# Kernel tuning notes

Hardware: AMD Instinct MI355X
Metric: run time of the kernel (lower is better)

Reference implementation:

```python
import jax, jax.numpy as jnp
import numpy as np

N, E, G = 2048, 65536, 32
F_ATOM, LAT, IN, ED, NB, L = 16, 64, 128, 32, 5, 5


def setup_inputs() -> dict:
    key = jax.random.key(0)
    ks = iter(jax.random.split(key, 64))
    nxt = lambda: next(ks)
    def w(shape):
        fan_in = shape[-2] if len(shape) >= 2 else 1
        return jax.random.normal(nxt(), shape, jnp.float32) / np.sqrt(fan_in)
    inp = {}
    inp['x'] = jax.random.normal(nxt(), (N, F_ATOM), jnp.float32)
    inp['t'] = jax.random.uniform(nxt(), (G, 1), jnp.float32)
    inp['z'] = jax.random.normal(nxt(), (N, LAT), jnp.float32)
    inp['edge_index'] = jax.random.randint(nxt(), (2, E), 0, N, jnp.int32)
    inp['edge_attr'] = jax.random.normal(nxt(), (E, NB), jnp.float32)
    inp['batch'] = jnp.sort(jax.random.randint(nxt(), (N,), 0, G, jnp.int32))
    inp['batch_edge_global'] = jax.random.randint(nxt(), (E,), 0, G, jnp.int32)
    # top-level dense layers
    inp['Wt_a'] = w((1, IN)); inp['bt_a'] = jnp.zeros((IN,))
    inp['Wt_b'] = w((1, ED)); inp['bt_b'] = jnp.zeros((ED,))
    inp['W_atom'] = w((F_ATOM, IN)); inp['b_atom'] = jnp.zeros((IN,))
    inp['W_bond'] = w((NB, ED)); inp['b_bond'] = jnp.zeros((ED,))
    inp['W_lat'] = w((LAT, IN)); inp['b_lat'] = jnp.zeros((IN,))
    inp['W_at'] = w((IN, IN)); inp['b_at'] = jnp.zeros((IN,))
    inp['W_bt'] = w((ED, ED)); inp['b_bt'] = jnp.zeros((ED,))
    # TopoEdgeGNN: L layers of edge-conditioned message passing with edge update
    inp['Wmsg'] = w((L, 2 * IN + ED, IN)); inp['bmsg'] = jnp.zeros((L, IN))
    inp['Wnode'] = w((L, 2 * IN, IN)); inp['bnode'] = jnp.zeros((L, IN))
    inp['Wedge'] = w((L, 2 * IN + ED, ED)); inp['bedge'] = jnp.zeros((L, ED))
    # prediction head
    inp['Wsh'] = w((IN, IN)); inp['bsh'] = jnp.zeros((IN,))
    inp['Wbm'] = w((ED, IN)); inp['bbm'] = jnp.zeros((IN,))
    inp['Wbl'] = w((IN, NB)); inp['bbl'] = jnp.zeros((NB,))
    inp['Wal'] = w((IN, F_ATOM + LAT)); inp['bal'] = jnp.zeros((F_ATOM + LAT,))
    return inp


def reference(x, t, z, edge_index, edge_attr, batch, batch_edge_global,
              Wt_a, bt_a, Wt_b, bt_b, W_atom, b_atom, W_bond, b_bond,
              W_lat, b_lat, W_at, b_at, W_bt, b_bt,
              Wmsg, bmsg, Wnode, bnode, Wedge, bedge,
              Wsh, bsh, Wbm, bbm, Wbl, bbl, Wal, bal):
    j, i = edge_index[0], edge_index[1]
    # time embeddings, gathered to nodes / edges
    ta = t @ Wt_a + bt_a            # [G, IN]
    tb = t @ Wt_b + bt_b            # [G, ED]
    tnode = ta[batch]               # [N, IN]
    tedge = tb[batch_edge_global]   # [E, ED]
    # node features
    s = x @ W_atom + b_atom
    s = (s + tnode) @ W_at + b_at
    s = s + (z @ W_lat + b_lat)
    # edge features
    e = edge_attr @ W_bond + b_bond
    e = (e + tedge) @ W_bt + b_bt
    # TopoEdgeGNN: message passing with residual node/edge updates
    for l in range(L):
        m = jax.nn.silu(jnp.concatenate([s[i], s[j], e], -1) @ Wmsg[l] + bmsg[l])  # [E, IN]
        agg = jax.ops.segment_sum(m, i, num_segments=N)                            # [N, IN]
        s = s + jax.nn.silu(jnp.concatenate([s, agg], -1) @ Wnode[l] + bnode[l])
        e = e + jax.nn.silu(jnp.concatenate([s[i], s[j], e], -1) @ Wedge[l] + bedge[l])
    # prediction head
    s2 = jax.nn.silu(s @ Wsh + bsh)
    al = s2 @ Wal + bal
    atoms_pred, latent_pred = al[:, :F_ATOM], al[:, F_ATOM:]
    # dense edge symmetrization: scatter edges into [N, N, ED], symmetrize, gather back
    e_dense = jnp.zeros((N, N, ED), e.dtype).at[j, i].set(e)
    e_dense = 0.5 * (e_dense + e_dense.transpose(1, 0, 2))
    e_sym = e_dense[j, i]           # [E, ED]
    f = jax.nn.silu(s2[i] + s2[j] + (e_sym @ Wbm + bbm))
    bonds_pred = f @ Wbl + bbl
    return latent_pred, atoms_pred, bonds_pred
```

## Files before the change

### kernel.cpp

```cpp
#include <hip/hip_runtime.h>
#include <hip/hip_bf16.h>

#define NN 2048
#define NE 65536
#define NG 32
#define CIN 128
#define CED 32
#define CLAT 64
#define CFA 16
#define CNB 5
#define NL 5

#define OFF_AT (NN * CLAT)
#define OFF_B  (NN * CLAT + NN * CFA)

typedef __attribute__((ext_vector_type(8))) short bf16x8;
typedef __attribute__((ext_vector_type(4))) float f32x4;

__device__ __forceinline__ float silu_f(float v) { return v / (1.0f + __expf(-v)); }
__device__ __forceinline__ short f2bs(float v) {
    __hip_bfloat16 h = __float2bfloat16(v);
    return *reinterpret_cast<short*>(&h);
}
__device__ __forceinline__ unsigned pack2(float a, float b) {
    return ((unsigned)(unsigned short)f2bs(b) << 16) | (unsigned short)f2bs(a);
}

__global__ __launch_bounds__(256) void k_prologue(
    const float* __restrict__ Wmsg, const float* __restrict__ Wedge,
    const float* __restrict__ Wnode, const float* __restrict__ Wsh,
    const float* __restrict__ Wal, const float* __restrict__ Wbm,
    short* __restrict__ Wpn, short* __restrict__ Wpsh,
    short* __restrict__ Wpal, short* __restrict__ Wpbm,
    short* __restrict__ Wproj, short* __restrict__ W3m, short* __restrict__ We3,
    const float* __restrict__ x, const float* __restrict__ t,
    const float* __restrict__ z, const int* __restrict__ batch,
    const float* __restrict__ Wt_a, const float* __restrict__ bt_a,
    const float* __restrict__ W_atom, const float* __restrict__ b_atom,
    const float* __restrict__ W_lat, const float* __restrict__ b_lat,
    const float* __restrict__ W_at, const float* __restrict__ b_at,
    float* __restrict__ s, short* __restrict__ s_bf,
    const int* __restrict__ ii, int* __restrict__ cnt)
{
    int b = blockIdx.x, tid = threadIdx.x;
    if (b < 960) {
        int idx = b * 256 + tid;
        int j = idx & 7, t0 = idx >> 3, lane = t0 & 63, tt = t0 >> 6;
        int kq = (lane >> 4) * 8 + j, n16 = lane & 15;
        if (idx < NL * 8 * 8 * 64 * 8) {
            int nt = tt & 7, kt = (tt >> 3) & 7, l = tt >> 6;
            Wpn[idx] = f2bs(Wnode[((size_t)l * 256 + kt * 32 + kq) * CIN + nt * 16 + n16]);
        }
        if (idx < 4 * 8 * 64 * 8) {
            int nt = tt & 7, kt = tt >> 3;
            Wpsh[idx] = f2bs(Wsh[(size_t)(kt * 32 + kq) * CIN + nt * 16 + n16]);
        }
        if (idx < 4 * 5 * 64 * 8) {
            int nt = tt % 5, kt = tt / 5;
            Wpal[idx] = f2bs(Wal[(size_t)(kt * 32 + kq) * 80 + nt * 16 + n16]);
        }
        if (idx < 8 * 64 * 8) {
            int nt = tt & 7;
            Wpbm[idx] = f2bs(Wbm[(size_t)kq * CIN + nt * 16 + n16]);
        }
        if (idx < 6 * 4 * 20 * 64 * 8) {
            int nt = tt % 20; int t2 = tt / 20; int kt = t2 & 3; int slot = t2 >> 2;
            int k = kt * 32 + kq;
            float v;
            if (nt < 16) {
                int msgl = slot % 5;
                int srcK = (nt < 8) ? k : 128 + k;
                int col = (nt & 7) * 16 + n16;
                v = Wmsg[((size_t)msgl * 288 + srcK) * CIN + col];
            } else {
                int edgel = (slot == 0) ? 0 : slot - 1;
                int srcK = (nt < 18) ? k : 128 + k;
                int col = (nt & 1) * 16 + n16;
                v = Wedge[((size_t)edgel * 288 + srcK) * CED + col];
            }
            Wproj[idx] = f2bs(v);
        }
        if (idx < NL * 8 * 64 * 8) {
            int nt = tt & 7, l = tt >> 3;
            W3m[idx] = f2bs(Wmsg[((size_t)l * 288 + 256 + kq) * CIN + nt * 16 + n16]);
        }
        if (idx < NL * 2 * 64 * 8) {
            int nt = tt & 1, l = tt >> 1;
            We3[idx] = f2bs(Wedge[((size_t)l * 288 + 256 + kq) * CED + nt * 16 + n16]);
        }
    } else if (b < 1088) {
        __shared__ float xs[16 * CFA];
        __shared__ float zs[16 * CLAT];
        __shared__ float tmp[16 * CIN];
        __shared__ float tv[16];
        int nb0 = (b - 960) * 16;
        int c = tid & 127, h = tid >> 7;
        if (tid < 16 * CFA / 4) ((float4*)xs)[tid] = ((const float4*)x)[nb0 * (CFA / 4) + tid];
        if (tid < 16 * CLAT / 4) ((float4*)zs)[tid] = ((const float4*)z)[nb0 * (CLAT / 4) + tid];
        if (tid < 16) tv[tid] = t[batch[nb0 + tid]];
        __syncthreads();
        float wta = Wt_a[c], base0 = b_atom[c] + bt_a[c];
        float acc[8];
#pragma unroll
        for (int q = 0; q < 8; q++) acc[q] = base0 + tv[h * 8 + q] * wta;
        for (int k = 0; k < CFA; k++) {
            float w = W_atom[k * CIN + c];
#pragma unroll
            for (int q = 0; q < 8; q++) acc[q] += xs[(h * 8 + q) * CFA + k] * w;
        }
#pragma unroll
        for (int q = 0; q < 8; q++) tmp[(h * 8 + q) * CIN + c] = acc[q];
        __syncthreads();
        float base1 = b_at[c] + b_lat[c];
        float acc2[8];
#pragma unroll
        for (int q = 0; q < 8; q++) acc2[q] = base1;
        for (int k4 = 0; k4 < CIN / 4; k4++) {
            float w0 = W_at[(4 * k4 + 0) * CIN + c], w1 = W_at[(4 * k4 + 1) * CIN + c];
            float w2 = W_at[(4 * k4 + 2) * CIN + c], w3 = W_at[(4 * k4 + 3) * CIN + c];
#pragma unroll
            for (int q = 0; q < 8; q++) {
                float4 f = *(const float4*)&tmp[(h * 8 + q) * CIN + 4 * k4];
                acc2[q] += f.x * w0 + f.y * w1 + f.z * w2 + f.w * w3;
            }
        }
        for (int k4 = 0; k4 < CLAT / 4; k4++) {
            float w0 = W_lat[(4 * k4 + 0) * CIN + c], w1 = W_lat[(4 * k4 + 1) * CIN + c];
            float w2 = W_lat[(4 * k4 + 2) * CIN + c], w3 = W_lat[(4 * k4 + 3) * CIN + c];
#pragma unroll
            for (int q = 0; q < 8; q++) {
                float4 f = *(const float4*)&zs[(h * 8 + q) * CLAT + 4 * k4];
                acc2[q] += f.x * w0 + f.y * w1 + f.z * w2 + f.w * w3;
            }
        }
#pragma unroll
        for (int q = 0; q < 8; q++) {
            int nd = nb0 + h * 8 + q;
            s[(size_t)nd * CIN + c] = acc2[q];
            s_bf[(size_t)nd * CIN + c] = f2bs(acc2[q]);
        }
    } else {
        int base = (b - 1088) * 1024;
#pragma unroll
        for (int q = 0; q < 4; q++) {
            int k = base + q * 256 + tid;
            atomicAdd(&cnt[ii[k]], 1);
        }
    }
}

__global__ __launch_bounds__(256) void k_prefix(const int* __restrict__ cnt, int* __restrict__ rowpos)
{
    __shared__ int part[256];
    int tid = threadIdx.x;
    int loc[8], sum = 0;
#pragma unroll
    for (int q = 0; q < 8; q++) { loc[q] = cnt[tid * 8 + q]; sum += loc[q]; }
    part[tid] = sum;
    __syncthreads();
    if (tid == 0) {
        int r = 0;
        for (int i = 0; i < 256; i++) { int v = part[i]; part[i] = r; r += v; }
    }
    __syncthreads();
    int r = part[tid];
#pragma unroll
    for (int q = 0; q < 8; q++) { rowpos[tid * 8 + q] = r; r += loc[q]; }
}

__global__ void k_perm(const int* __restrict__ ii, const int* __restrict__ jj,
                       int* __restrict__ rowpos, int* __restrict__ invp,
                       int* __restrict__ i_s, int* __restrict__ j_s)
{
    int k = blockIdx.x * 256 + threadIdx.x;
    int iv = ii[k];
    int p = atomicAdd(&rowpos[iv], 1);
    invp[k] = p;
    i_s[p] = iv;
    j_s[p] = jj[k];
}

__global__ __launch_bounds__(256) void k_init_e(
    const float* __restrict__ ea, const float* __restrict__ t,
    const int* __restrict__ beg, const int* __restrict__ jj, const int* __restrict__ ii,
    const int* __restrict__ invp,
    const float* __restrict__ Wt_b, const float* __restrict__ bt_b,
    const float* __restrict__ W_bond, const float* __restrict__ b_bond,
    const float* __restrict__ W_bt, const float* __restrict__ b_bt,
    float* __restrict__ e, short* __restrict__ e_bf, int* __restrict__ map)
{
    __shared__ float eas[64 * 5];
    __shared__ float tv[64];
    __shared__ int sp[64];
    __shared__ float tmp[64][33];
    __shared__ float wbt[32 * 32];
    __shared__ float wbond[5 * 32];
    __shared__ float cb[32], wtb[32], bbt2[32];
    int tid = threadIdx.x;
    int k0 = blockIdx.x * 64;
    for (int idx = tid; idx < 320; idx += 256) eas[idx] = ea[(size_t)k0 * 5 + idx];
    if (tid < 64) { tv[tid] = t[beg[k0 + tid]]; sp[tid] = invp[k0 + tid]; }
    for (int idx = tid; idx < 1024; idx += 256) wbt[idx] = W_bt[idx];
    if (tid < 160) wbond[tid] = W_bond[tid];
    if (tid < 32) { cb[tid] = b_bond[tid] + bt_b[tid]; wtb[tid] = Wt_b[tid]; bbt2[tid] = b_bt[tid]; }
    __syncthreads();
    int ch = tid & 31, eg = tid >> 5;
#pragma unroll
    for (int q = 0; q < 8; q++) {
        int le = eg * 8 + q;
        float acc = cb[ch] + tv[le] * wtb[ch];
#pragma unroll
        for (int bb = 0; bb < CNB; bb++) acc += eas[le * 5 + bb] * wbond[bb * 32 + ch];
        tmp[le][ch] = acc;
    }
    __syncthreads();
#pragma unroll
    for (int q = 0; q < 8; q++) {
        int le = eg * 8 + q;
        float acc2 = bbt2[ch];
        for (int d = 0; d < 32; d++) acc2 += tmp[le][d] * wbt[d * 32 + ch];
        size_t ix = (size_t)sp[le] * CED + ch;
        e[ix] = acc2;
        e_bf[ix] = f2bs(acc2);
        if (ch == 0) {
            int k = k0 + le;
            atomicMax(&map[(size_t)jj[k] * NN + ii[k]], k);
        }
    }
}

template<bool DO_NODE>
__global__ __launch_bounds__(256) void k_node_proj(
    float* __restrict__ s, short* __restrict__ s_bf, float* __restrict__ agg,
    const short* __restrict__ Wpn_l, const float* __restrict__ bnode_l,
    const short* __restrict__ Wproj, float* __restrict__ U, float* __restrict__ V,
    float* __restrict__ P, float* __restrict__ Q)
{
    __shared__ short feat[16 * 264];
    __shared__ short feat2[16 * 136];
    int tid = threadIdx.x;
    int nb0 = blockIdx.x * 16;
    int lane = tid & 63, w = tid >> 6;
    int quad = lane >> 4, n16 = lane & 15;

    if (DO_NODE) {
        {
            int kl = tid >> 4, c = tid & 15;
            *(uint4*)&feat[kl * 264 + c * 8] = ((const uint4*)s_bf)[(size_t)(nb0 + kl) * 16 + c];
        }
        for (int idx = tid; idx < 16 * 32; idx += 256) {
            int kl = idx >> 5, c = idx & 31;
            size_t gix = (size_t)(nb0 + kl) * 32 + c;
            float4 v = ((const float4*)agg)[gix];
            ((float4*)agg)[gix] = (float4){0.f, 0.f, 0.f, 0.f};
            uint2 p; p.x = pack2(v.x, v.y); p.y = pack2(v.z, v.w);
            *(uint2*)&feat[kl * 264 + 128 + 4 * c] = p;
        }
        __syncthreads();
        f32x4 acc[2];
        acc[0] = (f32x4){0.f, 0.f, 0.f, 0.f};
        acc[1] = (f32x4){0.f, 0.f, 0.f, 0.f};
        const short* fbase = feat + n16 * 264 + quad * 8;
#pragma unroll
        for (int kt = 0; kt < 8; kt++) {
            bf16x8 a = *(const bf16x8*)(fbase + kt * 32);
#pragma unroll
            for (int n2 = 0; n2 < 2; n2++) {
                int nt = w * 2 + n2;
                bf16x8 b = *(const bf16x8*)(Wpn_l + ((size_t)(kt * 8 + nt) * 64 + lane) * 8);
                acc[n2] = __builtin_amdgcn_mfma_f32_16x16x32_bf16(a, b, acc[n2], 0, 0, 0);
            }
        }
#pragma unroll
        for (int n2 = 0; n2 < 2; n2++) {
            int col = (w * 2 + n2) * 16 + n16;
            float bb = bnode_l[col];
#pragma unroll
            for (int r = 0; r < 4; r++) {
                int row = quad * 4 + r;
                size_t ix = (size_t)(nb0 + row) * CIN + col;
                float v = s[ix] + silu_f(acc[n2][r] + bb);
                s[ix] = v;
                short bv = f2bs(v);
                s_bf[ix] = bv;
                feat2[row * 136 + col] = bv;
            }
        }
        __syncthreads();
    } else {
        int kl = tid >> 4, c = tid & 15;
        *(uint4*)&feat2[kl * 136 + c * 8] = ((const uint4*)s_bf)[(size_t)(nb0 + kl) * 16 + c];
        __syncthreads();
    }

    f32x4 accp[5];
#pragma unroll
    for (int t2 = 0; t2 < 5; t2++) accp[t2] = (f32x4){0.f, 0.f, 0.f, 0.f};
    const short* abase = feat2 + n16 * 136 + quad * 8;
#pragma unroll
    for (int kt = 0; kt < 4; kt++) {
        bf16x8 a = *(const bf16x8*)(abase + kt * 32);
#pragma unroll
        for (int n5 = 0; n5 < 5; n5++) {
            int nt = w * 5 + n5;
            bf16x8 b = *(const bf16x8*)(Wproj + ((size_t)(kt * 20 + nt) * 64 + lane) * 8);
            accp[n5] = __builtin_amdgcn_mfma_f32_16x16x32_bf16(a, b, accp[n5], 0, 0, 0);
        }
    }
#pragma unroll
    for (int n5 = 0; n5 < 5; n5++) {
        int nt = w * 5 + n5;
#pragma unroll
        for (int r = 0; r < 4; r++) {
            int node = nb0 + quad * 4 + r;
            float v = accp[n5][r];
            if (nt < 8)       U[(size_t)node * CIN + nt * 16 + n16] = v;
            else if (nt < 16) V[(size_t)node * CIN + (nt - 8) * 16 + n16] = v;
            else if (nt < 18) P[(size_t)node * CED + (nt - 16) * 16 + n16] = v;
            else              Q[(size_t)node * CED + (nt - 18) * 16 + n16] = v;
        }
    }
}

template<bool DO_EDGE, bool DO_MSG>
__global__ __launch_bounds__(256) void k_em(
    const short* __restrict__ e_bf_in,
    const int* __restrict__ i_s, const int* __restrict__ j_s,
    const short* __restrict__ We3p, const float* __restrict__ bedge,
    const float* __restrict__ P, const float* __restrict__ Q,
    float* __restrict__ e, short* __restrict__ e_bf,
    const short* __restrict__ W3mp, const float* __restrict__ bmsg,
    const float* __restrict__ U, const float* __restrict__ V,
    float* __restrict__ agg)
{
    __shared__ short feat_e[64 * 40];
    __shared__ float uv[64 * 132];
    __shared__ float pq[64 * 36];
    __shared__ int sii[64], sjj[64];
    int tid = threadIdx.x;
    int e0 = blockIdx.x * 64;
    if (tid < 64) sii[tid] = i_s[e0 + tid];
    else if (tid < 128) sjj[tid - 64] = j_s[e0 + tid - 64];
    __syncthreads();
    {
        int kl = tid >> 2, c = tid & 3;
        uint4 v = ((const uint4*)e_bf_in)[(size_t)e0 * 4 + tid];
        *(uint4*)&feat_e[kl * 40 + c * 8] = v;
    }
    if (DO_EDGE) {
        for (int idx = tid; idx < 64 * 8; idx += 256) {
            int kl = idx >> 3, c = idx & 7;
            float4 a = ((const float4*)P)[(size_t)sii[kl] * 8 + c];
            float4 b = ((const float4*)Q)[(size_t)sjj[kl] * 8 + c];
            *(float4*)&pq[kl * 36 + 4 * c] = (float4){a.x + b.x, a.y + b.y, a.z + b.z, a.w + b.w};
        }
    }
    if (DO_MSG) {
        for (int idx = tid; idx < 64 * 32; idx += 256) {
            int kl = idx >> 5, c = idx & 31;
            float4 a = ((const float4*)U)[(size_t)sii[kl] * 32 + c];
            float4 b = ((const float4*)V)[(size_t)sjj[kl] * 32 + c];
            *(float4*)&uv[kl * 132 + 4 * c] = (float4){a.x + b.x, a.y + b.y, a.z + b.z, a.w + b.w};
        }
    }
    __syncthreads();
    int lane = tid & 63, w = tid >> 6;
    int quad = lane >> 4, n16 = lane & 15;
    const short* abase = feat_e + (w * 16 + n16) * 40 + quad * 8;
    bf16x8 a = *(const bf16x8*)abase;

    if (DO_EDGE) {
        f32x4 acc_e[2];
        acc_e[0] = (f32x4){0.f, 0.f, 0.f, 0.f};
        acc_e[1] = (f32x4){0.f, 0.f, 0.f, 0.f};
#pragma unroll
        for (int nt = 0; nt < 2; nt++) {
            bf16x8 b = *(const bf16x8*)(We3p + ((size_t)(nt * 64 + lane)) * 8);
            acc_e[nt] = __builtin_amdgcn_mfma_f32_16x16x32_bf16(a, b, acc_e[nt], 0, 0, 0);
        }
#pragma unroll
        for (int nt = 0; nt < 2; nt++) {
            int ch = nt * 16 + n16;
            float bb = bedge[ch];
#pragma unroll
            for (int r = 0; r < 4; r++) {
                int el = w * 16 + quad * 4 + r;
                size_t ix = (size_t)(e0 + el) * CED + ch;
                float v = e[ix] + silu_f(acc_e[nt][r] + bb + pq[el * 36 + ch]);
                e[ix] = v;
                short bv = f2bs(v);
                e_bf[ix] = bv;
                feat_e[el * 40 + ch] = bv;
            }
        }
        a = *(const bf16x8*)abase;
    }

    if (DO_MSG) {
        f32x4 acc_m[8];
#pragma unroll
        for (int t2 = 0; t2 < 8; t2++) acc_m[t2] = (f32x4){0.f, 0.f, 0.f, 0.f};
#pragma unroll
        for (int nt = 0; nt < 8; nt++) {
            bf16x8 b = *(const bf16x8*)(W3mp + ((size_t)(nt * 64 + lane)) * 8);
            acc_m[nt] = __builtin_amdgcn_mfma_f32_16x16x32_bf16(a, b, acc_m[nt], 0, 0, 0);
        }
#pragma unroll
        for (int nt = 0; nt < 8; nt++) {
            int ch = nt * 16 + n16;
            float bb = bmsg[ch];
#pragma unroll
            for (int r = 0; r < 4; r++) {
                int el = w * 16 + quad * 4 + r;
                int lix = el * 132 + ch;
                float m = silu_f(acc_m[nt][r] + bb + uv[lix]);
                uv[lix] = m;
            }
        }
        __syncthreads();
        if (tid < 128) {
            int c = tid;
            float run = 0.f;
            int cur = sii[0];
            for (int r = 0; r < 64; r++) {
                int tg = sii[r];
                if (tg != cur) { atomicAdd(&agg[(size_t)cur * CIN + c], run); run = 0.f; cur = tg; }
                run += uv[r * 132 + c];
            }
            atomicAdd(&agg[(size_t)cur * CIN + c], run);
        }
    }
}

__global__ __launch_bounds__(256) void k_post_node_mfma(
    const short* __restrict__ s_bf,
    const short* __restrict__ Wpsh, const float* __restrict__ bsh,
    const short* __restrict__ Wpal, const float* __restrict__ bal,
    float* __restrict__ s2, float* __restrict__ out)
{
    __shared__ short feat[16 * 136];
    __shared__ short feat_s2[16 * 136];
    int tid = threadIdx.x;
    int nb0 = blockIdx.x * 16;
    int lane = tid & 63, w = tid >> 6;
    int quad = lane >> 4, n16 = lane & 15;
    {
        int kl = tid >> 4, c = tid & 15;
        *(uint4*)&feat[kl * 136 + c * 8] = ((const uint4*)s_bf)[(size_t)(nb0 + kl) * 16 + c];
    }
    __syncthreads();
    const short* fbase = feat + n16 * 136 + quad * 8;
    f32x4 acc[2];
    acc[0] = (f32x4){0.f, 0.f, 0.f, 0.f};
    acc[1] = (f32x4){0.f, 0.f, 0.f, 0.f};
#pragma unroll
    for (int kt = 0; kt < 4; kt++) {
        bf16x8 a = *(const bf16x8*)(fbase + kt * 32);
#pragma unroll
        for (int n2 = 0; n2 < 2; n2++) {
            int nt = w * 2 + n2;
            bf16x8 b = *(const bf16x8*)(Wpsh + ((size_t)(kt * 8 + nt) * 64 + lane) * 8);
            acc[n2] = __builtin_amdgcn_mfma_f32_16x16x32_bf16(a, b, acc[n2], 0, 0, 0);
        }
    }
#pragma unroll
    for (int n2 = 0; n2 < 2; n2++) {
        int col = (w * 2 + n2) * 16 + n16;
        float bb = bsh[col];
#pragma unroll
        for (int r = 0; r < 4; r++) {
            int row = quad * 4 + r;
            float v = silu_f(acc[n2][r] + bb);
            s2[(size_t)(nb0 + row) * CIN + col] = v;
            feat_s2[row * 136 + col] = f2bs(v);
        }
    }
    __syncthreads();
    const short* abase = feat_s2 + n16 * 136 + quad * 8;
    f32x4 acca[2];
    acca[0] = (f32x4){0.f, 0.f, 0.f, 0.f};
    acca[1] = (f32x4){0.f, 0.f, 0.f, 0.f};
    int nAl = (w == 0) ? 2 : 1;
    int ntl[2] = {w, 4};
#pragma unroll
    for (int kt = 0; kt < 4; kt++) {
        bf16x8 a = *(const bf16x8*)(abase + kt * 32);
#pragma unroll
        for (int q = 0; q < 2; q++) {
            if (q < nAl) {
                bf16x8 b = *(const bf16x8*)(Wpal + ((size_t)(kt * 5 + ntl[q]) * 64 + lane) * 8);
                acca[q] = __builtin_amdgcn_mfma_f32_16x16x32_bf16(a, b, acca[q], 0, 0, 0);
            }
        }
    }
#pragma unroll
    for (int q = 0; q < 2; q++) {
        if (q < nAl) {
            int col = ntl[q] * 16 + n16;
            float bb = bal[col];
#pragma unroll
            for (int r = 0; r < 4; r++) {
                int node = nb0 + quad * 4 + r;
                float v = acca[q][r] + bb;
                if (col < CFA) out[OFF_AT + node * CFA + col] = v;
                else           out[(size_t)node * CLAT + (col - CFA)] = v;
            }
        }
    }
}

__global__ __launch_bounds__(256) void k_post_edge_mfma(
    const float* __restrict__ s2, const float* __restrict__ e,
    const int* __restrict__ ii, const int* __restrict__ jj,
    const int* __restrict__ map, const int* __restrict__ invp,
    const short* __restrict__ Wpbm, const float* __restrict__ bbm,
    const float* __restrict__ Wbl, const float* __restrict__ bbl,
    float* __restrict__ out)
{
    __shared__ int sii[64], sjj[64], skf[64], skb[64];
    __shared__ short esym[64 * 40];
    __shared__ float sbias[64 * 132];
    int tid = threadIdx.x;
    int e0 = blockIdx.x * 64;
    if (tid < 64) sii[tid] = ii[e0 + tid];
    else if (tid < 128) sjj[tid - 64] = jj[e0 + tid - 64];
    __syncthreads();
    if (tid < 64) skf[tid] = invp[map[(size_t)sjj[tid] * NN + sii[tid]]];
    else if (tid < 128) {
        int m = map[(size_t)sii[tid - 64] * NN + sjj[tid - 64]];
        skb[tid - 64] = (m >= 0) ? invp[m] : -1;
    }
    __syncthreads();
    for (int idx = tid; idx < 64 * 8; idx += 256) {
        int kl = idx >> 3, c = idx & 7;
        float4 a = ((const float4*)e)[(size_t)skf[kl] * 8 + c];
        int kb = skb[kl];
        float4 b = {0.f, 0.f, 0.f, 0.f};
        if (kb >= 0) b = ((const float4*)e)[(size_t)kb * 8 + c];
        uint2 p; p.x = pack2(0.5f * (a.x + b.x), 0.5f * (a.y + b.y));
        p.y = pack2(0.5f * (a.z + b.z), 0.5f * (a.w + b.w));
        *(uint2*)&esym[kl * 40 + 4 * c] = p;
    }
    for (int idx = tid; idx < 64 * 32; idx += 256) {
        int kl = idx >> 5, c = idx & 31;
        float4 a = ((const float4*)s2)[(size_t)sii[kl] * 32 + c];
        float4 b = ((const float4*)s2)[(size_t)sjj[kl] * 32 + c];
        float4 v = {a.x + b.x, a.y + b.y, a.z + b.z, a.w + b.w};
        *(float4*)&sbias[kl * 132 + 4 * c] = v;
    }
    __syncthreads();
    int lane = tid & 63, w = tid >> 6;
    int quad = lane >> 4, n16 = lane & 15;
    bf16x8 a = *(const bf16x8*)(esym + (w * 16 + n16) * 40 + quad * 8);
    f32x4 acc[8];
#pragma unroll
    for (int nt = 0; nt < 8; nt++) {
        bf16x8 b = *(const bf16x8*)(Wpbm + ((size_t)nt * 64 + lane) * 8);
        f32x4 zero = {0.f, 0.f, 0.f, 0.f};
        acc[nt] = __builtin_amdgcn_mfma_f32_16x16x32_bf16(a, b, zero, 0, 0, 0);
    }
    float f[8][4];
#pragma unroll
    for (int nt = 0; nt < 8; nt++) {
        int col = nt * 16 + n16;
        float bb = bbm[col];
#pragma unroll
        for (int r = 0; r < 4; r++) {
            int row = w * 16 + quad * 4 + r;
            f[nt][r] = silu_f(acc[nt][r] + bb + sbias[row * 132 + col]);
        }
    }
    __syncthreads();
    float* fshT = sbias;
#pragma unroll
    for (int nt = 0; nt < 8; nt++) {
        int col = nt * 16 + n16;
#pragma unroll
        for (int r = 0; r < 4; r++) {
            int row = w * 16 + quad * 4 + r;
            fshT[col * 66 + row] = f[nt][r];
        }
    }
    __syncthreads();
    for (int idx = tid; idx < 64 * CNB; idx += 256) {
        int kl = idx / CNB, b = idx - kl * CNB;
        float acc3 = bbl[b];
        for (int d = 0; d < CIN; d++) acc3 += fshT[d * 66 + kl] * Wbl[d * CNB + b];
        out[OFF_B + (size_t)(e0 + kl) * CNB + b] = acc3;
    }
}

extern "C" void kernel_launch(void* const* d_in, const int* in_sizes, int n_in,
                              void* d_out, int out_size, void* d_ws, size_t ws_size,
                              hipStream_t stream) {
    const float* x      = (const float*)d_in[0];
    const float* t      = (const float*)d_in[1];
    const float* z      = (const float*)d_in[2];
    const int*   eidx   = (const int*)d_in[3];
    const int*   jj     = eidx;
    const int*   ii     = eidx + NE;
    const float* ea     = (const float*)d_in[4];
    const int*   batch  = (const int*)d_in[5];
    const int*   beg    = (const int*)d_in[6];
    const float* Wt_a   = (const float*)d_in[7];
    const float* bt_a   = (const float*)d_in[8];
    const float* Wt_b   = (const float*)d_in[9];
    const float* bt_b   = (const float*)d_in[10];
    const float* W_atom = (const float*)d_in[11];
    const float* b_atom = (const float*)d_in[12];
    const float* W_bond = (const float*)d_in[13];
    const float* b_bond = (const float*)d_in[14];
    const float* W_lat  = (const float*)d_in[15];
    const float* b_lat  = (const float*)d_in[16];
    const float* W_at   = (const float*)d_in[17];
    const float* b_at   = (const float*)d_in[18];
    const float* W_bt   = (const float*)d_in[19];
    const float* b_bt   = (const float*)d_in[20];
    const float* Wmsg   = (const float*)d_in[21];
    const float* bmsg   = (const float*)d_in[22];
    const float* Wnode  = (const float*)d_in[23];
    const float* bnode  = (const float*)d_in[24];
    const float* Wedge  = (const float*)d_in[25];
    const float* bedge  = (const float*)d_in[26];
    const float* Wsh    = (const float*)d_in[27];
    const float* bsh    = (const float*)d_in[28];
    const float* Wbm    = (const float*)d_in[29];
    const float* bbm    = (const float*)d_in[30];
    const float* Wbl    = (const float*)d_in[31];
    const float* bbl    = (const float*)d_in[32];
    const float* Wal    = (const float*)d_in[33];
    const float* bal    = (const float*)d_in[34];

    float* s      = (float*)d_ws;
    float* e      = s + (size_t)NN * CIN;
    float* agg    = e + (size_t)NE * CED;
    int*   cnt    = (int*)(agg + (size_t)NN * CIN);
    int*   rowpos = cnt + NN;
    int*   invp   = rowpos + NN;
    int*   i_s    = invp + NE;
    int*   j_s    = i_s + NE;
    float* s2     = (float*)(j_s + NE);
    float* U      = s2 + (size_t)NN * CIN;
    float* V      = U + (size_t)NN * CIN;
    float* P      = V + (size_t)NN * CIN;
    float* Q      = P + (size_t)NN * CED;
    int*   map    = (int*)(Q + (size_t)NN * CED);
    short* s_bf   = (short*)(map + (size_t)NN * NN);
    short* e_bf   = s_bf + (size_t)NN * CIN;
    short* Wpn    = e_bf + (size_t)NE * CED;
    short* Wpsh   = Wpn + (size_t)NL * 8 * 8 * 64 * 8;
    short* Wpal   = Wpsh + (size_t)4 * 8 * 64 * 8;
    short* Wpbm   = Wpal + (size_t)4 * 5 * 64 * 8;
    short* Wproj  = Wpbm + (size_t)8 * 64 * 8;
    short* W3m    = Wproj + (size_t)6 * 4 * 20 * 64 * 8;
    short* We3    = W3m + (size_t)NL * 8 * 64 * 8;
    float* out    = (float*)d_out;

    hipMemsetAsync(map, 0xFF, (size_t)NN * NN * sizeof(int), stream);
    hipMemsetAsync(agg, 0, ((size_t)NN * CIN + NN) * sizeof(float), stream);
    k_prologue<<<1152, 256, 0, stream>>>(Wmsg, Wedge, Wnode, Wsh, Wal, Wbm,
                                         Wpn, Wpsh, Wpal, Wpbm, Wproj, W3m, We3,
                                         x, t, z, batch, Wt_a, bt_a, W_atom, b_atom,
                                         W_lat, b_lat, W_at, b_at, s, s_bf, ii, cnt);
    k_prefix<<<1, 256, 0, stream>>>(cnt, rowpos);
    k_perm<<<NE / 256, 256, 0, stream>>>(ii, jj, rowpos, invp, i_s, j_s);
    k_init_e<<<NE / 64, 256, 0, stream>>>(ea, t, beg, jj, ii, invp, Wt_b, bt_b,
                                          W_bond, b_bond, W_bt, b_bt, e, e_bf, map);

    k_node_proj<false><<<NN / 16, 256, 0, stream>>>(s, s_bf, agg, nullptr, nullptr,
                                                    Wproj, U, V, P, Q);
    k_em<false, true><<<NE / 64, 256, 0, stream>>>(e_bf, i_s, j_s,
                                                   nullptr, nullptr, P, Q, e, e_bf,
                                                   W3m, bmsg, U, V, agg);
    for (int l = 0; l < NL; l++) {
        k_node_proj<true><<<NN / 16, 256, 0, stream>>>(s, s_bf, agg,
                                                       Wpn + (size_t)l * 8 * 8 * 64 * 8,
                                                       bnode + l * CIN,
                                                       Wproj + (size_t)(l + 1) * 4 * 20 * 64 * 8,
                                                       U, V, P, Q);
        if (l < NL - 1) {
            k_em<true, true><<<NE / 64, 256, 0, stream>>>(e_bf, i_s, j_s,
                                                          We3 + (size_t)l * 2 * 64 * 8,
                                                          bedge + l * CED, P, Q, e, e_bf,
                                                          W3m + (size_t)(l + 1) * 8 * 64 * 8,
                                                          bmsg + (l + 1) * CIN, U, V, agg);
        } else {
            k_em<true, false><<<NE / 64, 256, 0, stream>>>(e_bf, i_s, j_s,
                                                           We3 + (size_t)l * 2 * 64 * 8,
                                                           bedge + l * CED, P, Q, e, e_bf,
                                                           nullptr, nullptr, nullptr, nullptr, agg);
        }
    }
    k_post_node_mfma<<<NN / 16, 256, 0, stream>>>(s_bf, Wpsh, bsh, Wpal, bal, s2, out);
    k_post_edge_mfma<<<NE / 64, 256, 0, stream>>>(s2, e, ii, jj, map, invp,
                                                  Wpbm, bbm, Wbl, bbl, out);
}
```

Before: 383.8 us.

## Fuse all stages into one cooperative persistent kernel with grid syncs

Turns the chain of about fifteen kernel launches (prologue, prefix, permutation, edge init, per-layer node projection and edge/message kernels, post-processing) into device phase functions. These run inside one cooperative kernel of 256 persistent blocks, separated by grid-wide barriers. The goal is to remove per-launch overhead and inter-kernel gaps. The cost is that a fixed grid of 256 blocks must loop over tiles, which may lower occupancy. Each grid sync also adds overhead. If the cooperative launch fails, it falls back to the separate kernels.

Result: slower. 1.462 ms (+281.0%).

```diff
diff --git a/kernel.cpp b/kernel.cpp
--- a/kernel.cpp
+++ b/kernel.cpp
@@ -1,5 +1,6 @@
 #include <hip/hip_runtime.h>
 #include <hip/hip_bf16.h>
+#include <hip/hip_cooperative_groups.h>
 
 #define NN 2048
 #define NE 65536
@@ -10,6 +11,7 @@
 #define CFA 16
 #define CNB 5
 #define NL 5
+#define GRID 256
 
 #define OFF_AT (NN * CLAT)
 #define OFF_B  (NN * CLAT + NN * CFA)
@@ -26,44 +28,46 @@
     return ((unsigned)(unsigned short)f2bs(b) << 16) | (unsigned short)f2bs(a);
 }
 
-__global__ __launch_bounds__(256) void k_prologue(
-    const float* __restrict__ Wmsg, const float* __restrict__ Wedge,
-    const float* __restrict__ Wnode, const float* __restrict__ Wsh,
-    const float* __restrict__ Wal, const float* __restrict__ Wbm,
-    short* __restrict__ Wpn, short* __restrict__ Wpsh,
-    short* __restrict__ Wpal, short* __restrict__ Wpbm,
-    short* __restrict__ Wproj, short* __restrict__ W3m, short* __restrict__ We3,
-    const float* __restrict__ x, const float* __restrict__ t,
-    const float* __restrict__ z, const int* __restrict__ batch,
-    const float* __restrict__ Wt_a, const float* __restrict__ bt_a,
-    const float* __restrict__ W_atom, const float* __restrict__ b_atom,
-    const float* __restrict__ W_lat, const float* __restrict__ b_lat,
-    const float* __restrict__ W_at, const float* __restrict__ b_at,
-    float* __restrict__ s, short* __restrict__ s_bf,
-    const int* __restrict__ ii, int* __restrict__ cnt)
-{
-    int b = blockIdx.x, tid = threadIdx.x;
-    if (b < 960) {
-        int idx = b * 256 + tid;
+struct KArgs {
+    const float *x, *t, *z;
+    const int *jj, *ii;
+    const float *ea;
+    const int *batch, *beg;
+    const float *Wt_a, *bt_a, *Wt_b, *bt_b, *W_atom, *b_atom, *W_bond, *b_bond;
+    const float *W_lat, *b_lat, *W_at, *b_at, *W_bt, *b_bt;
+    const float *Wmsg, *bmsg, *Wnode, *bnode, *Wedge, *bedge;
+    const float *Wsh, *bsh, *Wbm, *bbm, *Wbl, *bbl, *Wal, *bal;
+    float *s, *e, *agg;
+    int *cnt, *rowpos, *invp, *i_s, *j_s;
+    float *s2, *U, *V, *P, *Q;
+    int *map;
+    short *s_bf, *e_bf;
+    short *Wpn, *Wpsh, *Wpal, *Wpbm, *Wproj, *W3m, *We3;
+    float *out;
+};
+
+__device__ __forceinline__ void phase_pack(const KArgs& a, int start, int stride)
+{
+    for (int idx = start; idx < 6 * 4 * 20 * 64 * 8; idx += stride) {
         int j = idx & 7, t0 = idx >> 3, lane = t0 & 63, tt = t0 >> 6;
         int kq = (lane >> 4) * 8 + j, n16 = lane & 15;
         if (idx < NL * 8 * 8 * 64 * 8) {
             int nt = tt & 7, kt = (tt >> 3) & 7, l = tt >> 6;
-            Wpn[idx] = f2bs(Wnode[((size_t)l * 256 + kt * 32 + kq) * CIN + nt * 16 + n16]);
+            a.Wpn[idx] = f2bs(a.Wnode[((size_t)l * 256 + kt * 32 + kq) * CIN + nt * 16 + n16]);
         }
         if (idx < 4 * 8 * 64 * 8) {
             int nt = tt & 7, kt = tt >> 3;
-            Wpsh[idx] = f2bs(Wsh[(size_t)(kt * 32 + kq) * CIN + nt * 16 + n16]);
+            a.Wpsh[idx] = f2bs(a.Wsh[(size_t)(kt * 32 + kq) * CIN + nt * 16 + n16]);
         }
         if (idx < 4 * 5 * 64 * 8) {
             int nt = tt % 5, kt = tt / 5;
-            Wpal[idx] = f2bs(Wal[(size_t)(kt * 32 + kq) * 80 + nt * 16 + n16]);
+            a.Wpal[idx] = f2bs(a.Wal[(size_t)(kt * 32 + kq) * 80 + nt * 16 + n16]);
         }
         if (idx < 8 * 64 * 8) {
             int nt = tt & 7;
-            Wpbm[idx] = f2bs(Wbm[(size_t)kq * CIN + nt * 16 + n16]);
-        }
-        if (idx < 6 * 4 * 20 * 64 * 8) {
+            a.Wpbm[idx] = f2bs(a.Wbm[(size_t)kq * CIN + nt * 16 + n16]);
+        }
+        {
             int nt = tt % 20; int t2 = tt / 20; int kt = t2 & 3; int slot = t2 >> 2;
             int k = kt * 32 + kq;
             float v;
@@ -71,138 +75,98 @@
                 int msgl = slot % 5;
                 int srcK = (nt < 8) ? k : 128 + k;
                 int col = (nt & 7) * 16 + n16;
-                v = Wmsg[((size_t)msgl * 288 + srcK) * CIN + col];
+                v = a.Wmsg[((size_t)msgl * 288 + srcK) * CIN + col];
             } else {
                 int edgel = (slot == 0) ? 0 : slot - 1;
                 int srcK = (nt < 18) ? k : 128 + k;
                 int col = (nt & 1) * 16 + n16;
-                v = Wedge[((size_t)edgel * 288 + srcK) * CED + col];
+                v = a.Wedge[((size_t)edgel * 288 + srcK) * CED + col];
             }
-            Wproj[idx] = f2bs(v);
+            a.Wproj[idx] = f2bs(v);
         }
         if (idx < NL * 8 * 64 * 8) {
             int nt = tt & 7, l = tt >> 3;
-            W3m[idx] = f2bs(Wmsg[((size_t)l * 288 + 256 + kq) * CIN + nt * 16 + n16]);
+            a.W3m[idx] = f2bs(a.Wmsg[((size_t)l * 288 + 256 + kq) * CIN + nt * 16 + n16]);
         }
         if (idx < NL * 2 * 64 * 8) {
             int nt = tt & 1, l = tt >> 1;
-            We3[idx] = f2bs(Wedge[((size_t)l * 288 + 256 + kq) * CED + nt * 16 + n16]);
-        }
-    } else if (b < 1088) {
-        __shared__ float xs[16 * CFA];
-        __shared__ float zs[16 * CLAT];
-        __shared__ float tmp[16 * CIN];
-        __shared__ float tv[16];
-        int nb0 = (b - 960) * 16;
-        int c = tid & 127, h = tid >> 7;
-        if (tid < 16 * CFA / 4) ((float4*)xs)[tid] = ((const float4*)x)[nb0 * (CFA / 4) + tid];
-        if (tid < 16 * CLAT / 4) ((float4*)zs)[tid] = ((const float4*)z)[nb0 * (CLAT / 4) + tid];
-        if (tid < 16) tv[tid] = t[batch[nb0 + tid]];
-        __syncthreads();
-        float wta = Wt_a[c], base0 = b_atom[c] + bt_a[c];
-        float acc[8];
-#pragma unroll
-        for (int q = 0; q < 8; q++) acc[q] = base0 + tv[h * 8 + q] * wta;
-        for (int k = 0; k < CFA; k++) {
-            float w = W_atom[k * CIN + c];
-#pragma unroll
-            for (int q = 0; q < 8; q++) acc[q] += xs[(h * 8 + q) * CFA + k] * w;
-        }
-#pragma unroll
-        for (int q = 0; q < 8; q++) tmp[(h * 8 + q) * CIN + c] = acc[q];
-        __syncthreads();
-        float base1 = b_at[c] + b_lat[c];
-        float acc2[8];
-#pragma unroll
-        for (int q = 0; q < 8; q++) acc2[q] = base1;
-        for (int k4 = 0; k4 < CIN / 4; k4++) {
-            float w0 = W_at[(4 * k4 + 0) * CIN + c], w1 = W_at[(4 * k4 + 1) * CIN + c];
-            float w2 = W_at[(4 * k4 + 2) * CIN + c], w3 = W_at[(4 * k4 + 3) * CIN + c];
-#pragma unroll
-            for (int q = 0; q < 8; q++) {
-                float4 f = *(const float4*)&tmp[(h * 8 + q) * CIN + 4 * k4];
-                acc2[q] += f.x * w0 + f.y * w1 + f.z * w2 + f.w * w3;
-            }
-        }
-        for (int k4 = 0; k4 < CLAT / 4; k4++) {
-            float w0 = W_lat[(4 * k4 + 0) * CIN + c], w1 = W_lat[(4 * k4 + 1) * CIN + c];
-            float w2 = W_lat[(4 * k4 + 2) * CIN + c], w3 = W_lat[(4 * k4 + 3) * CIN + c];
-#pragma unroll
-            for (int q = 0; q < 8; q++) {
-                float4 f = *(const float4*)&zs[(h * 8 + q) * CLAT + 4 * k4];
-                acc2[q] += f.x * w0 + f.y * w1 + f.z * w2 + f.w * w3;
-            }
-        }
+            a.We3[idx] = f2bs(a.Wedge[((size_t)l * 288 + 256 + kq) * CED + nt * 16 + n16]);
+        }
+    }
+}
+
+__device__ __forceinline__ void phase_init_s(const KArgs& a, char* smem, int tile, int tid)
+{
+    float* xs  = (float*)smem;
+    float* zs  = (float*)(smem + 1024);
+    float* tmp = (float*)(smem + 5120);
+    float* tv  = (float*)(smem + 13312);
+    int nb0 = tile * 16;
+    int c = tid & 127, h = tid >> 7;
+    if (tid < 16 * CFA / 4) ((float4*)xs)[tid] = ((const float4*)a.x)[nb0 * (CFA / 4) + tid];
+    if (tid < 16 * CLAT / 4) ((float4*)zs)[tid] = ((const float4*)a.z)[nb0 * (CLAT / 4) + tid];
+    if (tid < 16) tv[tid] = a.t[a.batch[nb0 + tid]];
+    __syncthreads();
+    float wta = a.Wt_a[c], base0 = a.b_atom[c] + a.bt_a[c];
+    float acc[8];
+#pragma unroll
+    for (int q = 0; q < 8; q++) acc[q] = base0 + tv[h * 8 + q] * wta;
+    for (int k = 0; k < CFA; k++) {
+        float w = a.W_atom[k * CIN + c];
+#pragma unroll
+        for (int q = 0; q < 8; q++) acc[q] += xs[(h * 8 + q) * CFA + k] * w;
+    }
+#pragma unroll
+    for (int q = 0; q < 8; q++) tmp[(h * 8 + q) * CIN + c] = acc[q];
+    __syncthreads();
+    float base1 = a.b_at[c] + a.b_lat[c];
+    float acc2[8];
+#pragma unroll
+    for (int q = 0; q < 8; q++) acc2[q] = base1;
+    for (int k4 = 0; k4 < CIN / 4; k4++) {
+        float w0 = a.W_at[(4 * k4 + 0) * CIN + c], w1 = a.W_at[(4 * k4 + 1) * CIN + c];
+        float w2 = a.W_at[(4 * k4 + 2) * CIN + c], w3 = a.W_at[(4 * k4 + 3) * CIN + c];
 #pragma unroll
         for (int q = 0; q < 8; q++) {
-            int nd = nb0 + h * 8 + q;
-            s[(size_t)nd * CIN + c] = acc2[q];
-            s_bf[(size_t)nd * CIN + c] = f2bs(acc2[q]);
-        }
-    } else {
-        int base = (b - 1088) * 1024;
-#pragma unroll
-        for (int q = 0; q < 4; q++) {
-            int k = base + q * 256 + tid;
-            atomicAdd(&cnt[ii[k]], 1);
-        }
-    }
-}
-
-__global__ __launch_bounds__(256) void k_prefix(const int* __restrict__ cnt, int* __restrict__ rowpos)
-{
-    __shared__ int part[256];
-    int tid = threadIdx.x;
-    int loc[8], sum = 0;
-#pragma unroll
-    for (int q = 0; q < 8; q++) { loc[q] = cnt[tid * 8 + q]; sum += loc[q]; }
-    part[tid] = sum;
-    __syncthreads();
-    if (tid == 0) {
-        int r = 0;
-        for (int i = 0; i < 256; i++) { int v = part[i]; part[i] = r; r += v; }
-    }
-    __syncthreads();
-    int r = part[tid];
-#pragma unroll
-    for (int q = 0; q < 8; q++) { rowpos[tid * 8 + q] = r; r += loc[q]; }
-}
-
-__global__ void k_perm(const int* __restrict__ ii, const int* __restrict__ jj,
-                       int* __restrict__ rowpos, int* __restrict__ invp,
-                       int* __restrict__ i_s, int* __restrict__ j_s)
-{
-    int k = blockIdx.x * 256 + threadIdx.x;
-    int iv = ii[k];
-    int p = atomicAdd(&rowpos[iv], 1);
-    invp[k] = p;
-    i_s[p] = iv;
-    j_s[p] = jj[k];
-}
-
-__global__ __launch_bounds__(256) void k_init_e(
-    const float* __restrict__ ea, const float* __restrict__ t,
-    const int* __restrict__ beg, const int* __restrict__ jj, const int* __restrict__ ii,
-    const int* __restrict__ invp,
-    const float* __restrict__ Wt_b, const float* __restrict__ bt_b,
-    const float* __restrict__ W_bond, const float* __restrict__ b_bond,
-    const float* __restrict__ W_bt, const float* __restrict__ b_bt,
-    float* __restrict__ e, short* __restrict__ e_bf, int* __restrict__ map)
-{
-    __shared__ float eas[64 * 5];
-    __shared__ float tv[64];
-    __shared__ int sp[64];
-    __shared__ float tmp[64][33];
-    __shared__ float wbt[32 * 32];
-    __shared__ float wbond[5 * 32];
-    __shared__ float cb[32], wtb[32], bbt2[32];
-    int tid = threadIdx.x;
-    int k0 = blockIdx.x * 64;
-    for (int idx = tid; idx < 320; idx += 256) eas[idx] = ea[(size_t)k0 * 5 + idx];
-    if (tid < 64) { tv[tid] = t[beg[k0 + tid]]; sp[tid] = invp[k0 + tid]; }
-    for (int idx = tid; idx < 1024; idx += 256) wbt[idx] = W_bt[idx];
-    if (tid < 160) wbond[tid] = W_bond[tid];
-    if (tid < 32) { cb[tid] = b_bond[tid] + bt_b[tid]; wtb[tid] = Wt_b[tid]; bbt2[tid] = b_bt[tid]; }
+            float4 f = *(const float4*)&tmp[(h * 8 + q) * CIN + 4 * k4];
+            acc2[q] += f.x * w0 + f.y * w1 + f.z * w2 + f.w * w3;
+        }
+    }
+    for (int k4 = 0; k4 < CLAT / 4; k4++) {
+        float w0 = a.W_lat[(4 * k4 + 0) * CIN + c], w1 = a.W_lat[(4 * k4 + 1) * CIN + c];
+        float w2 = a.W_lat[(4 * k4 + 2) * CIN + c], w3 = a.W_lat[(4 * k4 + 3) * CIN + c];
+#pragma unroll
+        for (int q = 0; q < 8; q++) {
+            float4 f = *(const float4*)&zs[(h * 8 + q) * CLAT + 4 * k4];
+            acc2[q] += f.x * w0 + f.y * w1 + f.z * w2 + f.w * w3;
+        }
+    }
+#pragma unroll
+    for (int q = 0; q < 8; q++) {
+        int nd = nb0 + h * 8 + q;
+        a.s[(size_t)nd * CIN + c] = acc2[q];
+        a.s_bf[(size_t)nd * CIN + c] = f2bs(acc2[q]);
+    }
+    __syncthreads();
+}
+
+__device__ __forceinline__ void phase_init_e(const KArgs& a, char* smem, int tb, int tid)
+{
+    float* eas   = (float*)smem;
+    float* tv    = (float*)(smem + 1280);
+    int*   sp    = (int*)(smem + 1536);
+    float* tmp   = (float*)(smem + 1792);
+    float* wbt   = (float*)(smem + 10240);
+    float* wbond = (float*)(smem + 14336);
+    float* cb    = (float*)(smem + 14976);
+    float* wtb   = (float*)(smem + 15104);
+    float* bbt2  = (float*)(smem + 15232);
+    int k0 = tb * 64;
+    for (int idx = tid; idx < 320; idx += 256) eas[idx] = a.ea[(size_t)k0 * 5 + idx];
+    if (tid < 64) { tv[tid] = a.t[a.beg[k0 + tid]]; sp[tid] = a.invp[k0 + tid]; }
+    for (int idx = tid; idx < 1024; idx += 256) wbt[idx] = a.W_bt[idx];
+    if (tid < 160) wbond[tid] = a.W_bond[tid];
+    if (tid < 32) { cb[tid] = a.b_bond[tid] + a.bt_b[tid]; wtb[tid] = a.Wt_b[tid]; bbt2[tid] = a.b_bt[tid]; }
     __syncthreads();
     int ch = tid & 31, eg = tid >> 5;
 #pragma unroll
@@ -211,48 +175,43 @@
         float acc = cb[ch] + tv[le] * wtb[ch];
 #pragma unroll
         for (int bb = 0; bb < CNB; bb++) acc += eas[le * 5 + bb] * wbond[bb * 32 + ch];
-        tmp[le][ch] = acc;
+        tmp[le * 33 + ch] = acc;
     }
     __syncthreads();
 #pragma unroll
     for (int q = 0; q < 8; q++) {
         int le = eg * 8 + q;
         float acc2 = bbt2[ch];
-        for (int d = 0; d < 32; d++) acc2 += tmp[le][d] * wbt[d * 32 + ch];
+        for (int d = 0; d < 32; d++) acc2 += tmp[le * 33 + d] * wbt[d * 32 + ch];
         size_t ix = (size_t)sp[le] * CED + ch;
-        e[ix] = acc2;
-        e_bf[ix] = f2bs(acc2);
+        a.e[ix] = acc2;
+        a.e_bf[ix] = f2bs(acc2);
         if (ch == 0) {
             int k = k0 + le;
-            atomicMax(&map[(size_t)jj[k] * NN + ii[k]], k);
-        }
-    }
-}
-
-template<bool DO_NODE>
-__global__ __launch_bounds__(256) void k_node_proj(
-    float* __restrict__ s, short* __restrict__ s_bf, float* __restrict__ agg,
-    const short* __restrict__ Wpn_l, const float* __restrict__ bnode_l,
-    const short* __restrict__ Wproj, float* __restrict__ U, float* __restrict__ V,
-    float* __restrict__ P, float* __restrict__ Q)
-{
-    __shared__ short feat[16 * 264];
-    __shared__ short feat2[16 * 136];
-    int tid = threadIdx.x;
-    int nb0 = blockIdx.x * 16;
+            atomicMax(&a.map[(size_t)a.jj[k] * NN + a.ii[k]], k);
+        }
+    }
+    __syncthreads();
+}
+
+__device__ __forceinline__ void phase_node_proj(
+    const KArgs& a, char* smem, int tile, int tid, bool DO_NODE,
+    const short* Wpn_l, const float* bnode_l, const short* Wproj_slot)
+{
+    short* feat  = (short*)smem;
+    short* feat2 = (short*)(smem + 8448);
+    int nb0 = tile * 16;
     int lane = tid & 63, w = tid >> 6;
     int quad = lane >> 4, n16 = lane & 15;
 
     if (DO_NODE) {
-        {
-            int kl = tid >> 4, c = tid & 15;
-            *(uint4*)&feat[kl * 264 + c * 8] = ((const uint4*)s_bf)[(size_t)(nb0 + kl) * 16 + c];
-        }
+        { int kl = tid >> 4, c = tid & 15;
+          *(uint4*)&feat[kl * 264 + c * 8] = ((const uint4*)a.s_bf)[(size_t)(nb0 + kl) * 16 + c]; }
         for (int idx = tid; idx < 16 * 32; idx += 256) {
             int kl = idx >> 5, c = idx & 31;
             size_t gix = (size_t)(nb0 + kl) * 32 + c;
-            float4 v = ((const float4*)agg)[gix];
-            ((float4*)agg)[gix] = (float4){0.f, 0.f, 0.f, 0.f};
+            float4 v = ((const float4*)a.agg)[gix];
+            ((float4*)a.agg)[gix] = (float4){0.f, 0.f, 0.f, 0.f};
             uint2 p; p.x = pack2(v.x, v.y); p.y = pack2(v.z, v.w);
             *(uint2*)&feat[kl * 264 + 128 + 4 * c] = p;
         }
@@ -263,12 +222,12 @@
         const short* fbase = feat + n16 * 264 + quad * 8;
 #pragma unroll
         for (int kt = 0; kt < 8; kt++) {
-            bf16x8 a = *(const bf16x8*)(fbase + kt * 32);
+            bf16x8 av = *(const bf16x8*)(fbase + kt * 32);
 #pragma unroll
             for (int n2 = 0; n2 < 2; n2++) {
                 int nt = w * 2 + n2;
                 bf16x8 b = *(const bf16x8*)(Wpn_l + ((size_t)(kt * 8 + nt) * 64 + lane) * 8);
-                acc[n2] = __builtin_amdgcn_mfma_f32_16x16x32_bf16(a, b, acc[n2], 0, 0, 0);
+                acc[n2] = __builtin_amdgcn_mfma_f32_16x16x32_bf16(av, b, acc[n2], 0, 0, 0);
             }
         }
 #pragma unroll
@@ -279,17 +238,17 @@
             for (int r = 0; r < 4; r++) {
                 int row = quad * 4 + r;
                 size_t ix = (size_t)(nb0 + row) * CIN + col;
-                float v = s[ix] + silu_f(acc[n2][r] + bb);
-                s[ix] = v;
+                float v = a.s[ix] + silu_f(acc[n2][r] + bb);
+                a.s[ix] = v;
                 short bv = f2bs(v);
-                s_bf[ix] = bv;
+                a.s_bf[ix] = bv;
                 feat2[row * 136 + col] = bv;
             }
         }
         __syncthreads();
     } else {
         int kl = tid >> 4, c = tid & 15;
-        *(uint4*)&feat2[kl * 136 + c * 8] = ((const uint4*)s_bf)[(size_t)(nb0 + kl) * 16 + c];
+        *(uint4*)&feat2[kl * 136 + c * 8] = ((const uint4*)a.s_bf)[(size_t)(nb0 + kl) * 16 + c];
         __syncthreads();
     }
 
@@ -299,12 +258,12 @@
     const short* abase = feat2 + n16 * 136 + quad * 8;
 #pragma unroll
     for (int kt = 0; kt < 4; kt++) {
-        bf16x8 a = *(const bf16x8*)(abase + kt * 32);
+        bf16x8 av = *(const bf16x8*)(abase + kt * 32);
 #pragma unroll
         for (int n5 = 0; n5 < 5; n5++) {
             int nt = w * 5 + n5;
-            bf16x8 b = *(const bf16x8*)(Wproj + ((size_t)(kt * 20 + nt) * 64 + lane) * 8);
-            accp[n5] = __builtin_amdgcn_mfma_f32_16x16x32_bf16(a, b, accp[n5], 0, 0, 0);
+            bf16x8 b = *(const bf16x8*)(Wproj_slot + ((size_t)(kt * 20 + nt) * 64 + lane) * 8);
+            accp[n5] = __builtin_amdgcn_mfma_f32_16x16x32_bf16(av, b, accp[n5], 0, 0, 0);
         }
     }
 #pragma unroll
@@ -312,62 +271,54 @@
         int nt = w * 5 + n5;
 #pragma unroll
         for (int r = 0; r < 4; r++) {
-            int node = nb0 + quad * 4 + r;
+            int node = tile * 16 + quad * 4 + r;
             float v = accp[n5][r];
-            if (nt < 8)       U[(size_t)node * CIN + nt * 16 + n16] = v;
-            else if (nt < 16) V[(size_t)node * CIN + (nt - 8) * 16 + n16] = v;
-            else if (nt < 18) P[(size_t)node * CED + (nt - 16) * 16 + n16] = v;
-            else              Q[(size_t)node * CED + (nt - 18) * 16 + n16] = v;
-        }
-    }
-}
-
-template<bool DO_EDGE, bool DO_MSG>
-__global__ __launch_bounds__(256) void k_em(
-    const short* __restrict__ e_bf_in,
-    const int* __restrict__ i_s, const int* __restrict__ j_s,
-    const short* __restrict__ We3p, const float* __restrict__ bedge,
-    const float* __restrict__ P, const float* __restrict__ Q,
-    float* __restrict__ e, short* __restrict__ e_bf,
-    const short* __restrict__ W3mp, const float* __restrict__ bmsg,
-    const float* __restrict__ U, const float* __restrict__ V,
-    float* __restrict__ agg)
-{
-    __shared__ short feat_e[64 * 40];
-    __shared__ float uv[64 * 132];
-    __shared__ float pq[64 * 36];
-    __shared__ int sii[64], sjj[64];
-    int tid = threadIdx.x;
-    int e0 = blockIdx.x * 64;
-    if (tid < 64) sii[tid] = i_s[e0 + tid];
-    else if (tid < 128) sjj[tid - 64] = j_s[e0 + tid - 64];
-    __syncthreads();
-    {
-        int kl = tid >> 2, c = tid & 3;
-        uint4 v = ((const uint4*)e_bf_in)[(size_t)e0 * 4 + tid];
-        *(uint4*)&feat_e[kl * 40 + c * 8] = v;
-    }
+            if (nt < 8)       a.U[(size_t)node * CIN + nt * 16 + n16] = v;
+            else if (nt < 16) a.V[(size_t)node * CIN + (nt - 8) * 16 + n16] = v;
+            else if (nt < 18) a.P[(size_t)node * CED + (nt - 16) * 16 + n16] = v;
+            else              a.Q[(size_t)node * CED + (nt - 18) * 16 + n16] = v;
+        }
+    }
+    __syncthreads();
+}
+
+__device__ __forceinline__ void phase_em(
+    const KArgs& a, char* smem, int tb, int tid, bool DO_EDGE, bool DO_MSG,
+    const short* We3p, const float* bedge_l, const short* W3mp, const float* bmsg_l)
+{
+    short* feat_e = (short*)smem;
+    float* uv     = (float*)(smem + 5120);
+    float* pq     = (float*)(smem + 38912);
+    int*   sii    = (int*)(smem + 48128);
+    int*   sjj    = (int*)(smem + 48384);
+    int e0 = tb * 64;
+    if (tid < 64) sii[tid] = a.i_s[e0 + tid];
+    else if (tid < 128) sjj[tid - 64] = a.j_s[e0 + tid - 64];
+    __syncthreads();
+    { int kl = tid >> 2, c = tid & 3;
+      uint4 v = ((const uint4*)a.e_bf)[(size_t)e0 * 4 + tid];
+      *(uint4*)&feat_e[kl * 40 + c * 8] = v; }
     if (DO_EDGE) {
         for (int idx = tid; idx < 64 * 8; idx += 256) {
             int kl = idx >> 3, c = idx & 7;
-            float4 a = ((const float4*)P)[(size_t)sii[kl] * 8 + c];
-            float4 b = ((const float4*)Q)[(size_t)sjj[kl] * 8 + c];
-            *(float4*)&pq[kl * 36 + 4 * c] = (float4){a.x + b.x, a.y + b.y, a.z + b.z, a.w + b.w};
+            float4 av = ((const float4*)a.P)[(size_t)sii[kl] * 8 + c];
+            float4 bv = ((const float4*)a.Q)[(size_t)sjj[kl] * 8 + c];
+            *(float4*)&pq[kl * 36 + 4 * c] = (float4){av.x + bv.x, av.y + bv.y, av.z + bv.z, av.w + bv.w};
         }
     }
     if (DO_MSG) {
         for (int idx = tid; idx < 64 * 32; idx += 256) {
             int kl = idx >> 5, c = idx & 31;
-            float4 a = ((const float4*)U)[(size_t)sii[kl] * 32 + c];
-            float4 b = ((const float4*)V)[(size_t)sjj[kl] * 32 + c];
-            *(float4*)&uv[kl * 132 + 4 * c] = (float4){a.x + b.x, a.y + b.y, a.z + b.z, a.w + b.w};
+            float4 av = ((const float4*)a.U)[(size_t)sii[kl] * 32 + c];
+            float4 bv = ((const float4*)a.V)[(size_t)sjj[kl] * 32 + c];
+            *(float4*)&uv[kl * 132 + 4 * c] = (float4){av.x + bv.x, av.y + bv.y, av.z + bv.z, av.w + bv.w};
         }
     }
     __syncthreads();
     int lane = tid & 63, w = tid >> 6;
     int quad = lane >> 4, n16 = lane & 15;
     const short* abase = feat_e + (w * 16 + n16) * 40 + quad * 8;
-    bf16x8 a = *(const bf16x8*)abase;
+    bf16x8 av = *(const bf16x8*)abase;
 
     if (DO_EDGE) {
         f32x4 acc_e[2];
@@ -376,24 +327,24 @@
 #pragma unroll
         for (int nt = 0; nt < 2; nt++) {
             bf16x8 b = *(const bf16x8*)(We3p + ((size_t)(nt * 64 + lane)) * 8);
-            acc_e[nt] = __builtin_amdgcn_mfma_f32_16x16x32_bf16(a, b, acc_e[nt], 0, 0, 0);
+            acc_e[nt] = __builtin_amdgcn_mfma_f32_16x16x32_bf16(av, b, acc_e[nt], 0, 0, 0);
         }
 #pragma unroll
         for (int nt = 0; nt < 2; nt++) {
             int ch = nt * 16 + n16;
-            float bb = bedge[ch];
+            float bb = bedge_l[ch];
 #pragma unroll
             for (int r = 0; r < 4; r++) {
                 int el = w * 16 + quad * 4 + r;
                 size_t ix = (size_t)(e0 + el) * CED + ch;
-                float v = e[ix] + silu_f(acc_e[nt][r] + bb + pq[el * 36 + ch]);
-                e[ix] = v;
+                float v = a.e[ix] + silu_f(acc_e[nt][r] + bb + pq[el * 36 + ch]);
+                a.e[ix] = v;
                 short bv = f2bs(v);
-                e_bf[ix] = bv;
+                a.e_bf[ix] = bv;
                 feat_e[el * 40 + ch] = bv;
             }
         }
-        a = *(const bf16x8*)abase;
+        av = *(const bf16x8*)abase;
     }
 
     if (DO_MSG) {
@@ -403,12 +354,12 @@
 #pragma unroll
         for (int nt = 0; nt < 8; nt++) {
             bf16x8 b = *(const bf16x8*)(W3mp + ((size_t)(nt * 64 + lane)) * 8);
-            acc_m[nt] = __builtin_amdgcn_mfma_f32_16x16x32_bf16(a, b, acc_m[nt], 0, 0, 0);
+            acc_m[nt] = __builtin_amdgcn_mfma_f32_16x16x32_bf16(av, b, acc_m[nt], 0, 0, 0);
         }
 #pragma unroll
         for (int nt = 0; nt < 8; nt++) {
             int ch = nt * 16 + n16;
-            float bb = bmsg[ch];
+            float bb = bmsg_l[ch];
 #pragma unroll
             for (int r = 0; r < 4; r++) {
                 int el = w * 16 + quad * 4 + r;
@@ -424,30 +375,24 @@
             int cur = sii[0];
             for (int r = 0; r < 64; r++) {
                 int tg = sii[r];
-                if (tg != cur) { atomicAdd(&agg[(size_t)cur * CIN + c], run); run = 0.f; cur = tg; }
+                if (tg != cur) { atomicAdd(&a.agg[(size_t)cur * CIN + c], run); run = 0.f; cur = tg; }
                 run += uv[r * 132 + c];
             }
-            atomicAdd(&agg[(size_t)cur * CIN + c], run);
-        }
-    }
-}
-
-__global__ __launch_bounds__(256) void k_post_node_mfma(
-    const short* __restrict__ s_bf,
-    const short* __restrict__ Wpsh, const float* __restrict__ bsh,
-    const short* __restrict__ Wpal, const float* __restrict__ bal,
-    float* __restrict__ s2, float* __restrict__ out)
-{
-    __shared__ short feat[16 * 136];
-    __shared__ short feat_s2[16 * 136];
-    int tid = threadIdx.x;
-    int nb0 = blockIdx.x * 16;
+            atomicAdd(&a.agg[(size_t)cur * CIN + c], run);
+        }
+    }
+    __syncthreads();
+}
+
+__device__ __forceinline__ void phase_post_node(const KArgs& a, char* smem, int tile, int tid)
+{
+    short* feat    = (short*)smem;
+    short* feat_s2 = (short*)(smem + 4352);
+    int nb0 = tile * 16;
     int lane = tid & 63, w = tid >> 6;
     int quad = lane >> 4, n16 = lane & 15;
-    {
-        int kl = tid >> 4, c = tid & 15;
-        *(uint4*)&feat[kl * 136 + c * 8] = ((const uint4*)s_bf)[(size_t)(nb0 + kl) * 16 + c];
-    }
+    { int kl = tid >> 4, c = tid & 15;
+      *(uint4*)&feat[kl * 136 + c * 8] = ((const uint4*)a.s_bf)[(size_t)(nb0 + kl) * 16 + c]; }
     __syncthreads();
     const short* fbase = feat + n16 * 136 + quad * 8;
     f32x4 acc[2];
@@ -455,23 +400,23 @@
     acc[1] = (f32x4){0.f, 0.f, 0.f, 0.f};
 #pragma unroll
     for (int kt = 0; kt < 4; kt++) {
-        bf16x8 a = *(const bf16x8*)(fbase + kt * 32);
+        bf16x8 av = *(const bf16x8*)(fbase + kt * 32);
 #pragma unroll
         for (int n2 = 0; n2 < 2; n2++) {
             int nt = w * 2 + n2;
-            bf16x8 b = *(const bf16x8*)(Wpsh + ((size_t)(kt * 8 + nt) * 64 + lane) * 8);
-            acc[n2] = __builtin_amdgcn_mfma_f32_16x16x32_bf16(a, b, acc[n2], 0, 0, 0);
+            bf16x8 b = *(const bf16x8*)(a.Wpsh + ((size_t)(kt * 8 + nt) * 64 + lane) * 8);
+            acc[n2] = __builtin_amdgcn_mfma_f32_16x16x32_bf16(av, b, acc[n2], 0, 0, 0);
         }
     }
 #pragma unroll
     for (int n2 = 0; n2 < 2; n2++) {
         int col = (w * 2 + n2) * 16 + n16;
-        float bb = bsh[col];
+        float bb = a.bsh[col];
 #pragma unroll
         for (int r = 0; r < 4; r++) {
             int row = quad * 4 + r;
             float v = silu_f(acc[n2][r] + bb);
-            s2[(size_t)(nb0 + row) * CIN + col] = v;
+            a.s2[(size_t)(nb0 + row) * CIN + col] = v;
             feat_s2[row * 136 + col] = f2bs(v);
         }
     }
@@ -484,12 +429,12 @@
     int ntl[2] = {w, 4};
 #pragma unroll
     for (int kt = 0; kt < 4; kt++) {
-        bf16x8 a = *(const bf16x8*)(abase + kt * 32);
+        bf16x8 av = *(const bf16x8*)(abase + kt * 32);
 #pragma unroll
         for (int q = 0; q < 2; q++) {
             if (q < nAl) {
-                bf16x8 b = *(const bf16x8*)(Wpal + ((size_t)(kt * 5 + ntl[q]) * 64 + lane) * 8);
-                acca[q] = __builtin_amdgcn_mfma_f32_16x16x32_bf16(a, b, acca[q], 0, 0, 0);
+                bf16x8 b = *(const bf16x8*)(a.Wpal + ((size_t)(kt * 5 + ntl[q]) * 64 + lane) * 8);
+                acca[q] = __builtin_amdgcn_mfma_f32_16x16x32_bf16(av, b, acca[q], 0, 0, 0);
             }
         }
     }
@@ -497,73 +442,69 @@
     for (int q = 0; q < 2; q++) {
         if (q < nAl) {
             int col = ntl[q] * 16 + n16;
-            float bb = bal[col];
+            float bb = a.bal[col];
 #pragma unroll
             for (int r = 0; r < 4; r++) {
                 int node = nb0 + quad * 4 + r;
                 float v = acca[q][r] + bb;
-                if (col < CFA) out[OFF_AT + node * CFA + col] = v;
-                else           out[(size_t)node * CLAT + (col - CFA)] = v;
+                if (col < CFA) a.out[OFF_AT + node * CFA + col] = v;
+                else           a.out[(size_t)node * CLAT + (col - CFA)] = v;
             }
         }
     }
-}
-
-__global__ __launch_bounds__(256) void k_post_edge_mfma(
-    const float* __restrict__ s2, const float* __restrict__ e,
-    const int* __restrict__ ii, const int* __restrict__ jj,
-    const int* __restrict__ map, const int* __restrict__ invp,
-    const short* __restrict__ Wpbm, const float* __restrict__ bbm,
-    const float* __restrict__ Wbl, const float* __restrict__ bbl,
-    float* __restrict__ out)
-{
-    __shared__ int sii[64], sjj[64], skf[64], skb[64];
-    __shared__ short esym[64 * 40];
-    __shared__ float sbias[64 * 132];
-    int tid = threadIdx.x;
-    int e0 = blockIdx.x * 64;
-    if (tid < 64) sii[tid] = ii[e0 + tid];
-    else if (tid < 128) sjj[tid - 64] = jj[e0 + tid - 64];
-    __syncthreads();
-    if (tid < 64) skf[tid] = invp[map[(size_t)sjj[tid] * NN + sii[tid]]];
+    __syncthreads();
+}
+
+__device__ __forceinline__ void phase_post_edge(const KArgs& a, char* smem, int tb, int tid)
+{
+    short* esym  = (short*)smem;
+    float* sbias = (float*)(smem + 5120);
+    int* sii = (int*)(smem + 38912);
+    int* sjj = (int*)(smem + 39168);
+    int* skf = (int*)(smem + 39424);
+    int* skb = (int*)(smem + 39680);
+    int e0 = tb * 64;
+    if (tid < 64) sii[tid] = a.ii[e0 + tid];
+    else if (tid < 128) sjj[tid - 64] = a.jj[e0 + tid - 64];
+    __syncthreads();
+    if (tid < 64) skf[tid] = a.invp[a.map[(size_t)sjj[tid] * NN + sii[tid]]];
     else if (tid < 128) {
-        int m = map[(size_t)sii[tid - 64] * NN + sjj[tid - 64]];
-        skb[tid - 64] = (m >= 0) ? invp[m] : -1;
+        int m = a.map[(size_t)sii[tid - 64] * NN + sjj[tid - 64]];
+        skb[tid - 64] = (m >= 0) ? a.invp[m] : -1;
     }
     __syncthreads();
     for (int idx = tid; idx < 64 * 8; idx += 256) {
         int kl = idx >> 3, c = idx & 7;
-        float4 a = ((const float4*)e)[(size_t)skf[kl] * 8 + c];
+        float4 av = ((const float4*)a.e)[(size_t)skf[kl] * 8 + c];
         int kb = skb[kl];
-        float4 b = {0.f, 0.f, 0.f, 0.f};
-        if (kb >= 0) b = ((const float4*)e)[(size_t)kb * 8 + c];
-        uint2 p; p.x = pack2(0.5f * (a.x + b.x), 0.5f * (a.y + b.y));
-        p.y = pack2(0.5f * (a.z + b.z), 0.5f * (a.w + b.w));
+        float4 bv = {0.f, 0.f, 0.f, 0.f};
+        if (kb >= 0) bv = ((const float4*)a.e)[(size_t)kb * 8 + c];
+        uint2 p; p.x = pack2(0.5f * (av.x + bv.x), 0.5f * (av.y + bv.y));
+        p.y = pack2(0.5f * (av.z + bv.z), 0.5f * (av.w + bv.w));
         *(uint2*)&esym[kl * 40 + 4 * c] = p;
     }
     for (int idx = tid; idx < 64 * 32; idx += 256) {
         int kl = idx >> 5, c = idx & 31;
-        float4 a = ((const float4*)s2)[(size_t)sii[kl] * 32 + c];
-        float4 b = ((const float4*)s2)[(size_t)sjj[kl] * 32 + c];
-        float4 v = {a.x + b.x, a.y + b.y, a.z + b.z, a.w + b.w};
-        *(float4*)&sbias[kl * 132 + 4 * c] = v;
+        float4 av = ((const float4*)a.s2)[(size_t)sii[kl] * 32 + c];
+        float4 bv = ((const float4*)a.s2)[(size_t)sjj[kl] * 32 + c];
+        *(float4*)&sbias[kl * 132 + 4 * c] = (float4){av.x + bv.x, av.y + bv.y, av.z + bv.z, av.w + bv.w};
     }
     __syncthreads();
     int lane = tid & 63, w = tid >> 6;
     int quad = lane >> 4, n16 = lane & 15;
-    bf16x8 a = *(const bf16x8*)(esym + (w * 16 + n16) * 40 + quad * 8);
+    bf16x8 av = *(const bf16x8*)(esym + (w * 16 + n16) * 40 + quad * 8);
     f32x4 acc[8];
 #pragma unroll
     for (int nt = 0; nt < 8; nt++) {
-        bf16x8 b = *(const bf16x8*)(Wpbm + ((size_t)nt * 64 + lane) * 8);
+        bf16x8 b = *(const bf16x8*)(a.Wpbm + ((size_t)nt * 64 + lane) * 8);
         f32x4 zero = {0.f, 0.f, 0.f, 0.f};
-        acc[nt] = __builtin_amdgcn_mfma_f32_16x16x32_bf16(a, b, zero, 0, 0, 0);
+        acc[nt] = __builtin_amdgcn_mfma_f32_16x16x32_bf16(av, b, zero, 0, 0, 0);
     }
     float f[8][4];
 #pragma unroll
     for (int nt = 0; nt < 8; nt++) {
         int col = nt * 16 + n16;
-        float bb = bbm[col];
+        float bb = a.bbm[col];
 #pragma unroll
         for (int r = 0; r < 4; r++) {
             int row = w * 16 + quad * 4 + r;
@@ -584,114 +525,235 @@
     __syncthreads();
     for (int idx = tid; idx < 64 * CNB; idx += 256) {
         int kl = idx / CNB, b = idx - kl * CNB;
-        float acc3 = bbl[b];
-        for (int d = 0; d < CIN; d++) acc3 += fshT[d * 66 + kl] * Wbl[d * CNB + b];
-        out[OFF_B + (size_t)(e0 + kl) * CNB + b] = acc3;
-    }
+        float acc3 = a.bbl[b];
+        for (int d = 0; d < CIN; d++) acc3 += fshT[d * 66 + kl] * a.Wbl[d * CNB + b];
+        a.out[OFF_B + (size_t)(e0 + kl) * CNB + b] = acc3;
+    }
+    __syncthreads();
+}
+
+__global__ __launch_bounds__(256) void k_mega(KArgs a)
+{
+    namespace cg = cooperative_groups;
+    cg::grid_group grid = cg::this_grid();
+    __shared__ __align__(16) char smem[48640];
+    int bid = blockIdx.x, tid = threadIdx.x;
+
+    phase_pack(a, bid * 256 + tid, GRID * 256);
+    if (bid < 128) phase_init_s(a, smem, bid, tid);
+    for (int k = bid * 256 + tid; k < NE; k += GRID * 256) atomicAdd(&a.cnt[a.ii[k]], 1);
+    __threadfence(); grid.sync();
+
+    if (bid == 0) {
+        int* part = (int*)smem;
+        int loc[8], sum = 0;
+#pragma unroll
+        for (int q = 0; q < 8; q++) { loc[q] = a.cnt[tid * 8 + q]; sum += loc[q]; }
+        part[tid] = sum;
+        __syncthreads();
+        if (tid == 0) { int r = 0; for (int i = 0; i < 256; i++) { int v = part[i]; part[i] = r; r += v; } }
+        __syncthreads();
+        int r = part[tid];
+#pragma unroll
+        for (int q = 0; q < 8; q++) { a.rowpos[tid * 8 + q] = r; r += loc[q]; }
+    }
+    __threadfence(); grid.sync();
+
+    for (int k = bid * 256 + tid; k < NE; k += GRID * 256) {
+        int iv = a.ii[k];
+        int p = atomicAdd(&a.rowpos[iv], 1);
+        a.invp[k] = p;
+        a.i_s[p] = iv;
+        a.j_s[p] = a.jj[k];
+    }
+    __threadfence(); grid.sync();
+
+    for (int tb = bid; tb < NE / 64; tb += GRID) phase_init_e(a, smem, tb, tid);
+    __threadfence(); grid.sync();
+
+    if (bid < 128) phase_node_proj(a, smem, bid, tid, false, nullptr, nullptr, a.Wproj);
+    __threadfence(); grid.sync();
+
+    for (int tb = bid; tb < NE / 64; tb += GRID)
+        phase_em(a, smem, tb, tid, false, true, nullptr, nullptr, a.W3m, a.bmsg);
+    __threadfence(); grid.sync();
+
+    for (int l = 0; l < NL; l++) {
+        if (bid < 128)
+            phase_node_proj(a, smem, bid, tid, true,
+                            a.Wpn + (size_t)l * 8 * 8 * 64 * 8, a.bnode + l * CIN,
+                            a.Wproj + (size_t)(l + 1) * 4 * 20 * 64 * 8);
+        __threadfence(); grid.sync();
+        bool dm = (l < NL - 1);
+        for (int tb = bid; tb < NE / 64; tb += GRID)
+            phase_em(a, smem, tb, tid, true, dm,
+                     a.We3 + (size_t)l * 2 * 64 * 8, a.bedge + l * CED,
+                     dm ? a.W3m + (size_t)(l + 1) * 8 * 64 * 8 : a.W3m,
+                     dm ? a.bmsg + (l + 1) * CIN : a.bmsg);
+        __threadfence(); grid.sync();
+    }
+
+    if (bid < 128) phase_post_node(a, smem, bid, tid);
+    __threadfence(); grid.sync();
+
+    for (int tb = bid; tb < NE / 64; tb += GRID) phase_post_edge(a, smem, tb, tid);
+}
+
+__global__ __launch_bounds__(256) void k_w_prologue(KArgs a)
+{
+    __shared__ __align__(16) char smem[13440];
+    int b = blockIdx.x, tid = threadIdx.x;
+    if (b < 960) phase_pack(a, b * 256 + tid, 960 * 256);
+    else if (b < 1088) phase_init_s(a, smem, b - 960, tid);
+    else {
+        int base = (b - 1088) * 1024;
+#pragma unroll
+        for (int q = 0; q < 4; q++) atomicAdd(&a.cnt[a.ii[base + q * 256 + tid]], 1);
+    }
+}
+__global__ __launch_bounds__(256) void k_w_prefix(KArgs a)
+{
+    __shared__ int part[256];
+    int tid = threadIdx.x;
+    int loc[8], sum = 0;
+#pragma unroll
+    for (int q = 0; q < 8; q++) { loc[q] = a.cnt[tid * 8 + q]; sum += loc[q]; }
+    part[tid] = sum;
+    __syncthreads();
+    if (tid == 0) { int r = 0; for (int i = 0; i < 256; i++) { int v = part[i]; part[i] = r; r += v; } }
+    __syncthreads();
+    int r = part[tid];
+#pragma unroll
+    for (int q = 0; q < 8; q++) { a.rowpos[tid * 8 + q] = r; r += loc[q]; }
+}
+__global__ void k_w_perm(KArgs a)
+{
+    int k = blockIdx.x * 256 + threadIdx.x;
+    int iv = a.ii[k];
+    int p = atomicAdd(&a.rowpos[iv], 1);
+    a.invp[k] = p;
+    a.i_s[p] = iv;
+    a.j_s[p] = a.jj[k];
+}
+__global__ __launch_bounds__(256) void k_w_init_e(KArgs a)
+{
+    __shared__ __align__(16) char smem[15360];
+    phase_init_e(a, smem, blockIdx.x, threadIdx.x);
+}
+__global__ __launch_bounds__(256) void k_w_node_proj(KArgs a, int donode, const short* Wpn_l,
+                                                     const float* bnode_l, const short* Wproj_slot)
+{
+    __shared__ __align__(16) char smem[12800];
+    phase_node_proj(a, smem, blockIdx.x, threadIdx.x, donode != 0, Wpn_l, bnode_l, Wproj_slot);
+}
+__global__ __launch_bounds__(256) void k_w_em(KArgs a, int de, int dm, const short* We3p,
+                                              const float* bedge_l, const short* W3mp, const float* bmsg_l)
+{
+    __shared__ __align__(16) char smem[48640];
+    phase_em(a, smem, blockIdx.x, threadIdx.x, de != 0, dm != 0, We3p, bedge_l, W3mp, bmsg_l);
+}
+__global__ __launch_bounds__(256) void k_w_post_node(KArgs a)
+{
+    __shared__ __align__(16) char smem[8704];
+    phase_post_node(a, smem, blockIdx.x, threadIdx.x);
+}
+__global__ __launch_bounds__(256) void k_w_post_edge(KArgs a)
+{
+    __shared__ __align__(16) char smem[39936];
+    phase_post_edge(a, smem, blockIdx.x, threadIdx.x);
 }
 
 extern "C" void kernel_launch(void* const* d_in, const int* in_sizes, int n_in,
                               void* d_out, int out_size, void* d_ws, size_t ws_size,
                               hipStream_t stream) {
-    const float* x      = (const float*)d_in[0];
-    const float* t      = (const float*)d_in[1];
-    const float* z      = (const float*)d_in[2];
-    const int*   eidx   = (const int*)d_in[3];
-    const int*   jj     = eidx;
-    const int*   ii     = eidx + NE;
-    const float* ea     = (const float*)d_in[4];
-    const int*   batch  = (const int*)d_in[5];
-    const int*   beg    = (const int*)d_in[6];
-    const float* Wt_a   = (const float*)d_in[7];
-    const float* bt_a   = (const float*)d_in[8];
-    const float* Wt_b   = (const float*)d_in[9];
-    const float* bt_b   = (const float*)d_in[10];
-    const float* W_atom = (const float*)d_in[11];
-    const float* b_atom = (const float*)d_in[12];
-    const float* W_bond = (const float*)d_in[13];
-    const float* b_bond = (const float*)d_in[14];
-    const float* W_lat  = (const float*)d_in[15];
-    const float* b_lat  = (const float*)d_in[16];
-    const float* W_at   = (const float*)d_in[17];
-    const float* b_at   = (const float*)d_in[18];
-    const float* W_bt   = (const float*)d_in[19];
-    const float* b_bt   = (const float*)d_in[20];
-    const float* Wmsg   = (const float*)d_in[21];
-    const float* bmsg   = (const float*)d_in[22];
-    const float* Wnode  = (const float*)d_in[23];
-    const float* bnode  = (const float*)d_in[24];
-    const float* Wedge  = (const float*)d_in[25];
-    const float* bedge  = (const float*)d_in[26];
-    const float* Wsh    = (const float*)d_in[27];
-    const float* bsh    = (const float*)d_in[28];
-    const float* Wbm    = (const float*)d_in[29];
-    const float* bbm    = (const float*)d_in[30];
-    const float* Wbl    = (const float*)d_in[31];
-    const float* bbl    = (const float*)d_in[32];
-    const float* Wal    = (const float*)d_in[33];
-    const float* bal    = (const float*)d_in[34];
-
-    float* s      = (float*)d_ws;
-    float* e      = s + (size_t)NN * CIN;
-    float* agg    = e + (size_t)NE * CED;
-    int*   cnt    = (int*)(agg + (size_t)NN * CIN);
-    int*   rowpos = cnt + NN;
-    int*   invp   = rowpos + NN;
-    int*   i_s    = invp + NE;
-    int*   j_s    = i_s + NE;
-    float* s2     = (float*)(j_s + NE);
-    float* U      = s2 + (size_t)NN * CIN;
-    float* V      = U + (size_t)NN * CIN;
-    float* P      = V + (size_t)NN * CIN;
-    float* Q      = P + (size_t)NN * CED;
-    int*   map    = (int*)(Q + (size_t)NN * CED);
-    short* s_bf   = (short*)(map + (size_t)NN * NN);
-    short* e_bf   = s_bf + (size_t)NN * CIN;
-    short* Wpn    = e_bf + (size_t)NE * CED;
-    short* Wpsh   = Wpn + (size_t)NL * 8 * 8 * 64 * 8;
-    short* Wpal   = Wpsh + (size_t)4 * 8 * 64 * 8;
-    short* Wpbm   = Wpal + (size_t)4 * 5 * 64 * 8;
-    short* Wproj  = Wpbm + (size_t)8 * 64 * 8;
-    short* W3m    = Wproj + (size_t)6 * 4 * 20 * 64 * 8;
-    short* We3    = W3m + (size_t)NL * 8 * 64 * 8;
-    float* out    = (float*)d_out;
-
-    hipMemsetAsync(map, 0xFF, (size_t)NN * NN * sizeof(int), stream);
-    hipMemsetAsync(agg, 0, ((size_t)NN * CIN + NN) * sizeof(float), stream);
-    k_prologue<<<1152, 256, 0, stream>>>(Wmsg, Wedge, Wnode, Wsh, Wal, Wbm,
-                                         Wpn, Wpsh, Wpal, Wpbm, Wproj, W3m, We3,
-                                         x, t, z, batch, Wt_a, bt_a, W_atom, b_atom,
-                                         W_lat, b_lat, W_at, b_at, s, s_bf, ii, cnt);
-    k_prefix<<<1, 256, 0, stream>>>(cnt, rowpos);
-    k_perm<<<NE / 256, 256, 0, stream>>>(ii, jj, rowpos, invp, i_s, j_s);
-    k_init_e<<<NE / 64, 256, 0, stream>>>(ea, t, beg, jj, ii, invp, Wt_b, bt_b,
-                                          W_bond, b_bond, W_bt, b_bt, e, e_bf, map);
-
-    k_node_proj<false><<<NN / 16, 256, 0, stream>>>(s, s_bf, agg, nullptr, nullptr,
-                                                    Wproj, U, V, P, Q);
-    k_em<false, true><<<NE / 64, 256, 0, stream>>>(e_bf, i_s, j_s,
-                                                   nullptr, nullptr, P, Q, e, e_bf,
-                                                   W3m, bmsg, U, V, agg);
-    for (int l = 0; l < NL; l++) {
-        k_node_proj<true><<<NN / 16, 256, 0, stream>>>(s, s_bf, agg,
-                                                       Wpn + (size_t)l * 8 * 8 * 64 * 8,
-                                                       bnode + l * CIN,
-                                                       Wproj + (size_t)(l + 1) * 4 * 20 * 64 * 8,
-                                                       U, V, P, Q);
-        if (l < NL - 1) {
-            k_em<true, true><<<NE / 64, 256, 0, stream>>>(e_bf, i_s, j_s,
-                                                          We3 + (size_t)l * 2 * 64 * 8,
-                                                          bedge + l * CED, P, Q, e, e_bf,
-                                                          W3m + (size_t)(l + 1) * 8 * 64 * 8,
-                                                          bmsg + (l + 1) * CIN, U, V, agg);
-        } else {
-            k_em<true, false><<<NE / 64, 256, 0, stream>>>(e_bf, i_s, j_s,
-                                                           We3 + (size_t)l * 2 * 64 * 8,
-                                                           bedge + l * CED, P, Q, e, e_bf,
-                                                           nullptr, nullptr, nullptr, nullptr, agg);
-        }
-    }
-    k_post_node_mfma<<<NN / 16, 256, 0, stream>>>(s_bf, Wpsh, bsh, Wpal, bal, s2, out);
-    k_post_edge_mfma<<<NE / 64, 256, 0, stream>>>(s2, e, ii, jj, map, invp,
-                                                  Wpbm, bbm, Wbl, bbl, out);
-}
+    KArgs a;
+    a.x      = (const float*)d_in[0];
+    a.t      = (const float*)d_in[1];
+    a.z      = (const float*)d_in[2];
+    const int* eidx = (const int*)d_in[3];
+    a.jj     = eidx;
+    a.ii     = eidx + NE;
+    a.ea     = (const float*)d_in[4];
+    a.batch  = (const int*)d_in[5];
+    a.beg    = (const int*)d_in[6];
+    a.Wt_a   = (const float*)d_in[7];
+    a.bt_a   = (const float*)d_in[8];
+    a.Wt_b   = (const float*)d_in[9];
+    a.bt_b   = (const float*)d_in[10];
+    a.W_atom = (const float*)d_in[11];
+    a.b_atom = (const float*)d_in[12];
+    a.W_bond = (const float*)d_in[13];
+    a.b_bond = (const float*)d_in[14];
+    a.W_lat  = (const float*)d_in[15];
+    a.b_lat  = (const float*)d_in[16];
+    a.W_at   = (const float*)d_in[17];
+    a.b_at   = (const float*)d_in[18];
+    a.W_bt   = (const float*)d_in[19];
+    a.b_bt   = (const float*)d_in[20];
+    a.Wmsg   = (const float*)d_in[21];
+    a.bmsg   = (const float*)d_in[22];
+    a.Wnode  = (const float*)d_in[23];
+    a.bnode  = (const float*)d_in[24];
+    a.Wedge  = (const float*)d_in[25];
+    a.bedge  = (const float*)d_in[26];
+    a.Wsh    = (const float*)d_in[27];
+    a.bsh    = (const float*)d_in[28];
+    a.Wbm    = (const float*)d_in[29];
+    a.bbm    = (const float*)d_in[30];
+    a.Wbl    = (const float*)d_in[31];
+    a.bbl    = (const float*)d_in[32];
+    a.Wal    = (const float*)d_in[33];
+    a.bal    = (const float*)d_in[34];
+
+    a.s      = (float*)d_ws;
+    a.e      = a.s + (size_t)NN * CIN;
+    a.agg    = a.e + (size_t)NE * CED;
+    a.cnt    = (int*)(a.agg + (size_t)NN * CIN);
+    a.rowpos = a.cnt + NN;
+    a.invp   = a.rowpos + NN;
+    a.i_s    = a.invp + NE;
+    a.j_s    = a.i_s + NE;
+    a.s2     = (float*)(a.j_s + NE);
+    a.U      = a.s2 + (size_t)NN * CIN;
+    a.V      = a.U + (size_t)NN * CIN;
+    a.P      = a.V + (size_t)NN * CIN;
+    a.Q      = a.P + (size_t)NN * CED;
+    a.map    = (int*)(a.Q + (size_t)NN * CED);
+    a.s_bf   = (short*)(a.map + (size_t)NN * NN);
+    a.e_bf   = a.s_bf + (size_t)NN * CIN;
+    a.Wpn    = a.e_bf + (size_t)NE * CED;
+    a.Wpsh   = a.Wpn + (size_t)NL * 8 * 8 * 64 * 8;
+    a.Wpal   = a.Wpsh + (size_t)4 * 8 * 64 * 8;
+    a.Wpbm   = a.Wpal + (size_t)4 * 5 * 64 * 8;
+    a.Wproj  = a.Wpbm + (size_t)8 * 64 * 8;
+    a.W3m    = a.Wproj + (size_t)6 * 4 * 20 * 64 * 8;
+    a.We3    = a.W3m + (size_t)NL * 8 * 64 * 8;
+    a.out    = (float*)d_out;
+
+    hipMemsetAsync(a.map, 0xFF, (size_t)NN * NN * sizeof(int), stream);
+    hipMemsetAsync(a.agg, 0, ((size_t)NN * CIN + NN) * sizeof(float), stream);
+
+    void* params[] = { (void*)&a };
+    hipError_t rc = hipLaunchCooperativeKernel((const void*)k_mega, dim3(GRID), dim3(256),
+                                               params, 0, stream);
+    if (rc != hipSuccess) {
+        k_w_prologue<<<1152, 256, 0, stream>>>(a);
+        k_w_prefix<<<1, 256, 0, stream>>>(a);
+        k_w_perm<<<NE / 256, 256, 0, stream>>>(a);
+        k_w_init_e<<<NE / 64, 256, 0, stream>>>(a);
+        k_w_node_proj<<<NN / 16, 256, 0, stream>>>(a, 0, nullptr, nullptr, a.Wproj);
+        k_w_em<<<NE / 64, 256, 0, stream>>>(a, 0, 1, nullptr, nullptr, a.W3m, a.bmsg);
+        for (int l = 0; l < NL; l++) {
+            k_w_node_proj<<<NN / 16, 256, 0, stream>>>(a, 1,
+                a.Wpn + (size_t)l * 8 * 8 * 64 * 8, a.bnode + l * CIN,
+                a.Wproj + (size_t)(l + 1) * 4 * 20 * 64 * 8);
+            int dm = (l < NL - 1) ? 1 : 0;
+            k_w_em<<<NE / 64, 256, 0, stream>>>(a, 1, dm,
+                a.We3 + (size_t)l * 2 * 64 * 8, a.bedge + l * CED,
+                dm ? a.W3m + (size_t)(l + 1) * 8 * 64 * 8 : a.W3m,
+                dm ? a.bmsg + (l + 1) * CIN : a.bmsg);
+        }
+        k_w_post_node<<<NN / 16, 256, 0, stream>>>(a);
+        k_w_post_edge<<<NE / 64, 256, 0, stream>>>(a);
+    }
+}
```
